# Performance work log

Measured on AMD Instinct MI355X. Metric: run time of the kernel, lower is better.

The kernel has to match this reference:

```python
import jax, jax.numpy as jnp
import numpy as np

B, N, D, H = 128, 32768, 768, 16
DH = D // H          # per-head hidden_size = memory_dim // num_heads = 48
BETA = 0.25          # scaling (inverse temperature)
STEPS = 5            # update_steps_max
TOPK = 4


def _ln(x, g, b):
    # torch nn.LayerNorm over last dim (biased variance, eps=1e-5), affine
    m = jnp.mean(x, axis=-1, keepdims=True)
    v = jnp.var(x, axis=-1, keepdims=True)
    return (x - m) * jax.lax.rsqrt(v + 1e-5) * g + b


def _l2norm(x):
    # F.normalize(x, dim=-1): x / max(||x||, 1e-12)
    n = jnp.linalg.norm(x, axis=-1, keepdims=True)
    return x / jnp.maximum(n, 1e-12)


def setup_inputs() -> dict:
    key = jax.random.key(0)
    ks = jax.random.split(key, 8)
    s = 0.05  # weight init scale to keep activations sane
    return {
        "query_embedding": jax.random.normal(ks[0], (B, D), jnp.float32),
        "memory_bank": jax.random.normal(ks[1], (N, D), jnp.float32),
        "ln_k_g": jnp.ones((D,), jnp.float32), "ln_k_b": jnp.zeros((D,), jnp.float32),
        "ln_q_g": jnp.ones((D,), jnp.float32), "ln_q_b": jnp.zeros((D,), jnp.float32),
        "ln_v_g": jnp.ones((D,), jnp.float32), "ln_v_b": jnp.zeros((D,), jnp.float32),
        "Wq": jax.random.normal(ks[2], (D, D), jnp.float32) * s, "bq": jnp.zeros((D,), jnp.float32),
        "Wk": jax.random.normal(ks[3], (D, D), jnp.float32) * s, "bk": jnp.zeros((D,), jnp.float32),
        "Wv": jax.random.normal(ks[4], (D, D), jnp.float32) * s, "bv": jnp.zeros((D,), jnp.float32),
        "Wo": jax.random.normal(ks[5], (D, D), jnp.float32) * s, "bo": jnp.zeros((D,), jnp.float32),
        "W1": jax.random.normal(ks[6], (D, D), jnp.float32) * s, "b1": jnp.zeros((D,), jnp.float32),
        "W2": jax.random.normal(ks[7], (D, D), jnp.float32) * s, "b2": jnp.zeros((D,), jnp.float32),
    }


def reference(query_embedding, memory_bank, ln_k_g, ln_k_b, ln_q_g, ln_q_b,
              ln_v_g, ln_v_b, Wq, bq, Wk, bk, Wv, bv, Wo, bo, W1, b1, W2, b2):
    # Affine LayerNorms on stored pattern, state pattern, pattern projection.
    # memory_bank is shared across the batch, so normalize/project it ONCE
    # instead of materializing the (B, N, D) expand from the torch code.
    stored = _ln(memory_bank, ln_k_g, ln_k_b)        # (N, D)
    state = _ln(query_embedding, ln_q_g, ln_q_b)     # (B, D) -- state pattern, seq len 1
    projp = _ln(memory_bank, ln_v_g, ln_v_b)         # (N, D)

    k = (stored @ Wk.T + bk).reshape(N, H, DH)       # (N, H, dh)
    v = (projp @ Wv.T + bv).reshape(N, H, DH)        # (N, H, dh)
    q = (state @ Wq.T + bq).reshape(B, H, DH)        # (B, H, dh)

    # Hopfield convergence: xi <- softmax(beta * xi K^T) K, repeated STEPS times
    def step(xi, _):
        attn = jax.nn.softmax(BETA * jnp.einsum('bhd,nhd->bhn', xi, k), axis=-1)
        return jnp.einsum('bhn,nhd->bhd', attn, k), None

    xi, _ = jax.lax.scan(step, q, None, length=STEPS)

    # Final readout against the (separately normalized) pattern projection V
    attn = jax.nn.softmax(BETA * jnp.einsum('bhd,nhd->bhn', xi, k), axis=-1)  # (B, H, N)
    converged = jnp.einsum('bhn,nhd->bhd', attn, v).reshape(B, D) @ Wo.T + bo  # (B, D)

    # Retrieval head: residual + MLP + cosine-sim logits + top-k
    combined = query_embedding + converged
    rq = jax.nn.relu(combined @ W1.T + b1) @ W2.T + b2
    logits = (_l2norm(rq) @ _l2norm(memory_bank).T) * 20.0   # (B, N)
    top_indices = jax.lax.top_k(logits, TOPK)[1]              # (B, TOPK)
    return top_indices, logits
```

## Files before the change

### kernel.cpp

```cpp
#include <hip/hip_runtime.h>
#include <math.h>

#define NTOT 32768
#define DMODEL 768
#define BSZ 128
#define NHEAD 16
#define DH 48
#define BETA 0.25f

typedef _Float16 f16;
typedef f16 f16x8 __attribute__((ext_vector_type(8)));
typedef f16 f16x4 __attribute__((ext_vector_type(4)));
typedef float f32x4 __attribute__((ext_vector_type(4)));

__global__ __launch_bounds__(256)
void row_stats(const float* __restrict__ X, int M, float* __restrict__ mean,
               float* __restrict__ rstd, float* __restrict__ l2inv) {
  const int row = blockIdx.x * 4 + (threadIdx.x >> 6);
  const int lane = threadIdx.x & 63;
  if (row >= M) return;
  const float* x = X + (size_t)row * DMODEL;
  float s = 0.f, s2 = 0.f;
  for (int i = lane; i < DMODEL; i += 64) {
    float v = x[i];
    s += v; s2 += v * v;
  }
#pragma unroll
  for (int off = 32; off; off >>= 1) {
    s  += __shfl_xor(s, off);
    s2 += __shfl_xor(s2, off);
  }
  if (lane == 0) {
    float mu = s * (1.f / DMODEL);
    float var = s2 * (1.f / DMODEL) - mu * mu;
    mean[row] = mu;
    rstd[row] = rsqrtf(var + 1e-5f);
    if (l2inv) l2inv[row] = 1.f / fmaxf(sqrtf(s2), 1e-12f);
  }
}

__global__ __launch_bounds__(256)
void split_ln(const float* __restrict__ X, const float* __restrict__ mean,
              const float* __restrict__ rstd, f16* __restrict__ hi,
              f16* __restrict__ lo) {
  const int i8 = blockIdx.x * 256 + threadIdx.x;
  const int row = i8 / 96;
  const float mu = mean[row], rs = rstd[row];
  const float* xp = X + (size_t)i8 * 8;
  const float4 a = *(const float4*)xp;
  const float4 b = *(const float4*)(xp + 4);
  const float x[8] = {a.x, a.y, a.z, a.w, b.x, b.y, b.z, b.w};
  f16x8 h, l;
#pragma unroll
  for (int j = 0; j < 8; j++) {
    const float s = (x[j] - mu) * rs;
    const f16 hv = (f16)s;
    h[j] = hv;
    l[j] = (f16)(s - (float)hv);
  }
  *(f16x8*)(hi + (size_t)i8 * 8) = h;
  *(f16x8*)(lo + (size_t)i8 * 8) = l;
}

__global__ __launch_bounds__(256)
void split_plain(const float* __restrict__ X, f16* __restrict__ hi,
                 f16* __restrict__ lo) {
  const int i8 = blockIdx.x * 256 + threadIdx.x;
  const float* xp = X + (size_t)i8 * 8;
  const float4 a = *(const float4*)xp;
  const float4 b = *(const float4*)(xp + 4);
  const float x[8] = {a.x, a.y, a.z, a.w, b.x, b.y, b.z, b.w};
  f16x8 h, l;
#pragma unroll
  for (int j = 0; j < 8; j++) {
    const f16 hv = (f16)x[j];
    h[j] = hv;
    l[j] = (f16)(x[j] - (float)hv);
  }
  *(f16x8*)(hi + (size_t)i8 * 8) = h;
  *(f16x8*)(lo + (size_t)i8 * 8) = l;
}

__global__ __launch_bounds__(256)
void prep_w(const float* __restrict__ Wk, const float* __restrict__ bk,
            const float* __restrict__ gk, const float* __restrict__ blnk,
            const float* __restrict__ Wv, const float* __restrict__ bv,
            const float* __restrict__ gv, const float* __restrict__ blnv,
            f16* __restrict__ Wc_hi, f16* __restrict__ Wc_lo,
            float* __restrict__ biasc) {
  const int o = blockIdx.x * 4 + (threadIdx.x >> 6);
  const int lane = threadIdx.x & 63;
  const bool isK = o < DMODEL;
  const float* W = isK ? (Wk + (size_t)o * DMODEL)
                       : (Wv + (size_t)(o - DMODEL) * DMODEL);
  const float* g   = isK ? gk : gv;
  const float* bln = isK ? blnk : blnv;
  float bacc = 0.f;
  for (int d = lane * 4; d < DMODEL; d += 256) {
    const float4 wv = *(const float4*)(W + d);
    const float4 g4 = *(const float4*)(g + d);
    const float4 b4 = *(const float4*)(bln + d);
    bacc += wv.x * b4.x + wv.y * b4.y + wv.z * b4.z + wv.w * b4.w;
    const float sv[4] = {wv.x * g4.x * 16.f, wv.y * g4.y * 16.f,
                         wv.z * g4.z * 16.f, wv.w * g4.w * 16.f};
    f16x4 h4, l4;
#pragma unroll
    for (int j = 0; j < 4; j++) {
      const f16 h = (f16)sv[j];
      h4[j] = h;
      l4[j] = (f16)(sv[j] - (float)h);
    }
    *(f16x4*)(Wc_hi + (size_t)o * DMODEL + d) = h4;
    *(f16x4*)(Wc_lo + (size_t)o * DMODEL + d) = l4;
  }
#pragma unroll
  for (int off = 32; off; off >>= 1) bacc += __shfl_xor(bacc, off);
  if (lane == 0) biasc[o] = (isK ? bk[o] : bv[o - DMODEL]) + bacc;
}

__global__ __launch_bounds__(256)
void proj_dual_v2(const f16* __restrict__ nh_hi, const f16* __restrict__ nh_lo,
                  const f16* __restrict__ Wc_hi, const f16* __restrict__ Wc_lo,
                  const float* __restrict__ biasc,
                  f16* __restrict__ k_hi, f16* __restrict__ k_lo,
                  f16* __restrict__ v_hi, f16* __restrict__ v_lo) {
  __shared__ __align__(16) f16 As[2][128][40];
  __shared__ __align__(16) f16 Bs[2][128][40];
  const int t = threadIdx.x;
  const int n0 = blockIdx.x * 128;
  const int m0 = blockIdx.y * 128;
  const int w = t >> 6, lane = t & 63;
  const int l15 = lane & 15, lq = lane >> 4;
  const int wm = w >> 1, wn = w & 1;
  const int sr = t >> 1, sh = t & 1;

  f32x4 acc[4][4];
#pragma unroll
  for (int a = 0; a < 4; a++)
#pragma unroll
    for (int b = 0; b < 4; b++)
#pragma unroll
      for (int r = 0; r < 4; r++) acc[a][b][r] = 0.f;

  for (int k0 = 0; k0 < DMODEL; k0 += 32) {
    __syncthreads();
    {
      const size_t aoff = (size_t)(m0 + sr) * DMODEL + k0 + sh * 16;
      f16x8 ah0 = *(const f16x8*)(nh_hi + aoff);
      f16x8 ah1 = *(const f16x8*)(nh_hi + aoff + 8);
      f16x8 al0 = *(const f16x8*)(nh_lo + aoff);
      f16x8 al1 = *(const f16x8*)(nh_lo + aoff + 8);
      *(f16x8*)&As[0][sr][sh * 16] = ah0;
      *(f16x8*)&As[0][sr][sh * 16 + 8] = ah1;
      *(f16x8*)&As[1][sr][sh * 16] = al0;
      *(f16x8*)&As[1][sr][sh * 16 + 8] = al1;
    }
    {
      const size_t boff = (size_t)(n0 + sr) * DMODEL + k0 + sh * 16;
      f16x8 bh0 = *(const f16x8*)(Wc_hi + boff);
      f16x8 bh1 = *(const f16x8*)(Wc_hi + boff + 8);
      f16x8 bl0 = *(const f16x8*)(Wc_lo + boff);
      f16x8 bl1 = *(const f16x8*)(Wc_lo + boff + 8);
      *(f16x8*)&Bs[0][sr][sh * 16] = bh0;
      *(f16x8*)&Bs[0][sr][sh * 16 + 8] = bh1;
      *(f16x8*)&Bs[1][sr][sh * 16] = bl0;
      *(f16x8*)&Bs[1][sr][sh * 16 + 8] = bl1;
    }
    __syncthreads();
    f16x8 nhh[4], nhl[4];
#pragma unroll
    for (int fm = 0; fm < 4; fm++) {
      const int row = wm * 64 + fm * 16 + l15;
      nhh[fm] = *(const f16x8*)&As[0][row][lq * 8];
      nhl[fm] = *(const f16x8*)&As[1][row][lq * 8];
    }
    f16x8 wh[4], wl[4];
#pragma unroll
    for (int fo = 0; fo < 4; fo++) {
      const int row = wn * 64 + fo * 16 + l15;
      wh[fo] = *(const f16x8*)&Bs[0][row][lq * 8];
      wl[fo] = *(const f16x8*)&Bs[1][row][lq * 8];
    }
#pragma unroll
    for (int fo = 0; fo < 4; fo++)
#pragma unroll
      for (int fm = 0; fm < 4; fm++) {
        f32x4 a = acc[fo][fm];
        a = __builtin_amdgcn_mfma_f32_16x16x32_f16(wh[fo], nhh[fm], a, 0, 0, 0);
        a = __builtin_amdgcn_mfma_f32_16x16x32_f16(wh[fo], nhl[fm], a, 0, 0, 0);
        a = __builtin_amdgcn_mfma_f32_16x16x32_f16(wl[fo], nhh[fm], a, 0, 0, 0);
        acc[fo][fm] = a;
      }
  }
  const int oc = n0 + wn * 64;
  const bool isK = oc < DMODEL;
  f16* oh = isK ? k_hi : v_hi;
  f16* ol = isK ? k_lo : v_lo;
  const int obase = (isK ? oc : oc - DMODEL) + lq * 4;
#pragma unroll
  for (int fo = 0; fo < 4; fo++) {
    const float4 bb = *(const float4*)(biasc + oc + fo * 16 + lq * 4);
    const float bbv[4] = {bb.x, bb.y, bb.z, bb.w};
    const int o = obase + fo * 16;
#pragma unroll
    for (int fm = 0; fm < 4; fm++) {
      const size_t moff = (size_t)(m0 + wm * 64 + fm * 16 + l15) * DMODEL + o;
      f16x4 h4, l4;
#pragma unroll
      for (int r = 0; r < 4; r++) {
        const float v = acc[fo][fm][r] * 0.0625f + bbv[r];
        const f16 h = (f16)v;
        h4[r] = h;
        l4[r] = (f16)(v - (float)h);
      }
      *(f16x4*)(oh + moff) = h4;
      *(f16x4*)(ol + moff) = l4;
    }
  }
}

__global__ __launch_bounds__(256)
void proj_dual_insplit(const float* __restrict__ mb, const float* __restrict__ mean,
                       const float* __restrict__ rstd,
                       const f16* __restrict__ Wc_hi, const f16* __restrict__ Wc_lo,
                       const float* __restrict__ biasc,
                       f16* __restrict__ k_hi, f16* __restrict__ k_lo,
                       f16* __restrict__ v_hi, f16* __restrict__ v_lo) {
  __shared__ __align__(16) f16 As[2][128][40];
  __shared__ __align__(16) f16 Bs[2][128][40];
  const int t = threadIdx.x;
  const int n0 = blockIdx.x * 128;
  const int m0 = blockIdx.y * 128;
  const int w = t >> 6, lane = t & 63;
  const int l15 = lane & 15, lq = lane >> 4;
  const int wm = w >> 1, wn = w & 1;
  const int sr = t >> 1, sh = t & 1;
  const float mu = mean[m0 + sr];
  const float rs = rstd[m0 + sr];
  f32x4 acc[4][4];
#pragma unroll
  for (int a = 0; a < 4; a++)
#pragma unroll
    for (int b = 0; b < 4; b++)
#pragma unroll
      for (int r = 0; r < 4; r++) acc[a][b][r] = 0.f;
  for (int k0 = 0; k0 < DMODEL; k0 += 32) {
    __syncthreads();
    {
      const float* ap = mb + (size_t)(m0 + sr) * DMODEL + k0 + sh * 16;
      float x[16];
#pragma unroll
      for (int c = 0; c < 4; c++) {
        const float4 v4 = *(const float4*)(ap + c * 4);
        x[c * 4 + 0] = v4.x; x[c * 4 + 1] = v4.y;
        x[c * 4 + 2] = v4.z; x[c * 4 + 3] = v4.w;
      }
      f16x8 h0, h1, l0, l1;
#pragma unroll
      for (int j = 0; j < 8; j++) {
        const float s = (x[j] - mu) * rs;
        const f16 h = (f16)s;
        h0[j] = h; l0[j] = (f16)(s - (float)h);
      }
#pragma unroll
      for (int j = 0; j < 8; j++) {
        const float s = (x[8 + j] - mu) * rs;
        const f16 h = (f16)s;
        h1[j] = h; l1[j] = (f16)(s - (float)h);
      }
      *(f16x8*)&As[0][sr][sh * 16] = h0;
      *(f16x8*)&As[0][sr][sh * 16 + 8] = h1;
      *(f16x8*)&As[1][sr][sh * 16] = l0;
      *(f16x8*)&As[1][sr][sh * 16 + 8] = l1;
    }
    {
      const size_t boff = (size_t)(n0 + sr) * DMODEL + k0 + sh * 16;
      f16x8 bh0 = *(const f16x8*)(Wc_hi + boff);
      f16x8 bh1 = *(const f16x8*)(Wc_hi + boff + 8);
      f16x8 bl0 = *(const f16x8*)(Wc_lo + boff);
      f16x8 bl1 = *(const f16x8*)(Wc_lo + boff + 8);
      *(f16x8*)&Bs[0][sr][sh * 16] = bh0;
      *(f16x8*)&Bs[0][sr][sh * 16 + 8] = bh1;
      *(f16x8*)&Bs[1][sr][sh * 16] = bl0;
      *(f16x8*)&Bs[1][sr][sh * 16 + 8] = bl1;
    }
    __syncthreads();
    f16x8 nhh[4], nhl[4];
#pragma unroll
    for (int fm = 0; fm < 4; fm++) {
      const int row = wm * 64 + fm * 16 + l15;
      nhh[fm] = *(const f16x8*)&As[0][row][lq * 8];
      nhl[fm] = *(const f16x8*)&As[1][row][lq * 8];
    }
    f16x8 wh[4], wl[4];
#pragma unroll
    for (int fo = 0; fo < 4; fo++) {
      const int row = wn * 64 + fo * 16 + l15;
      wh[fo] = *(const f16x8*)&Bs[0][row][lq * 8];
      wl[fo] = *(const f16x8*)&Bs[1][row][lq * 8];
    }
#pragma unroll
    for (int fo = 0; fo < 4; fo++)
#pragma unroll
      for (int fm = 0; fm < 4; fm++) {
        f32x4 a = acc[fo][fm];
        a = __builtin_amdgcn_mfma_f32_16x16x32_f16(wh[fo], nhh[fm], a, 0, 0, 0);
        a = __builtin_amdgcn_mfma_f32_16x16x32_f16(wh[fo], nhl[fm], a, 0, 0, 0);
        a = __builtin_amdgcn_mfma_f32_16x16x32_f16(wl[fo], nhh[fm], a, 0, 0, 0);
        acc[fo][fm] = a;
      }
  }
  const int oc = n0 + wn * 64;
  const bool isK = oc < DMODEL;
  f16* oh = isK ? k_hi : v_hi;
  f16* ol = isK ? k_lo : v_lo;
  const int obase = (isK ? oc : oc - DMODEL) + lq * 4;
#pragma unroll
  for (int fo = 0; fo < 4; fo++) {
    const float4 bb = *(const float4*)(biasc + oc + fo * 16 + lq * 4);
    const float bbv[4] = {bb.x, bb.y, bb.z, bb.w};
    const int o = obase + fo * 16;
#pragma unroll
    for (int fm = 0; fm < 4; fm++) {
      const size_t moff = (size_t)(m0 + wm * 64 + fm * 16 + l15) * DMODEL + o;
      f16x4 h4, l4;
#pragma unroll
      for (int r = 0; r < 4; r++) {
        const float v = acc[fo][fm][r] * 0.0625f + bbv[r];
        const f16 h = (f16)v;
        h4[r] = h;
        l4[r] = (f16)(v - (float)h);
      }
      *(f16x4*)(oh + moff) = h4;
      *(f16x4*)(ol + moff) = l4;
    }
  }
}

__global__ __launch_bounds__(256)
void logits_mfma(const f16* __restrict__ mb_hi, const f16* __restrict__ mb_lo,
                 const f16* __restrict__ rq_hi, const f16* __restrict__ rq_lo,
                 const float* __restrict__ ainv, const float* __restrict__ binv,
                 float* __restrict__ out) {
  __shared__ __align__(16) f16 As[2][128][40];
  __shared__ __align__(16) f16 Bs[2][128][40];
  const int t = threadIdx.x;
  const int n0 = blockIdx.x * 128;
  const int w = t >> 6, lane = t & 63;
  const int l15 = lane & 15, lq = lane >> 4;
  const int wb = w >> 1, wn = w & 1;
  const int sr = t >> 1, sh = t & 1;

  f32x4 acc[4][4];
#pragma unroll
  for (int a = 0; a < 4; a++)
#pragma unroll
    for (int b = 0; b < 4; b++)
#pragma unroll
      for (int r = 0; r < 4; r++) acc[a][b][r] = 0.f;

  for (int k0 = 0; k0 < DMODEL; k0 += 32) {
    __syncthreads();
    {
      const size_t aoff = (size_t)(n0 + sr) * DMODEL + k0 + sh * 16;
      f16x8 ah0 = *(const f16x8*)(mb_hi + aoff);
      f16x8 ah1 = *(const f16x8*)(mb_hi + aoff + 8);
      f16x8 al0 = *(const f16x8*)(mb_lo + aoff);
      f16x8 al1 = *(const f16x8*)(mb_lo + aoff + 8);
      *(f16x8*)&As[0][sr][sh * 16] = ah0;
      *(f16x8*)&As[0][sr][sh * 16 + 8] = ah1;
      *(f16x8*)&As[1][sr][sh * 16] = al0;
      *(f16x8*)&As[1][sr][sh * 16 + 8] = al1;
    }
    {
      const size_t boff = (size_t)sr * DMODEL + k0 + sh * 16;
      f16x8 bh0 = *(const f16x8*)(rq_hi + boff);
      f16x8 bh1 = *(const f16x8*)(rq_hi + boff + 8);
      f16x8 bl0 = *(const f16x8*)(rq_lo + boff);
      f16x8 bl1 = *(const f16x8*)(rq_lo + boff + 8);
      *(f16x8*)&Bs[0][sr][sh * 16] = bh0;
      *(f16x8*)&Bs[0][sr][sh * 16 + 8] = bh1;
      *(f16x8*)&Bs[1][sr][sh * 16] = bl0;
      *(f16x8*)&Bs[1][sr][sh * 16 + 8] = bl1;
    }
    __syncthreads();
    f16x8 ah[4], al[4];
#pragma unroll
    for (int fn = 0; fn < 4; fn++) {
      const int row = wn * 64 + fn * 16 + l15;
      ah[fn] = *(const f16x8*)&As[0][row][lq * 8];
      al[fn] = *(const f16x8*)&As[1][row][lq * 8];
    }
    f16x8 bh[4], bl[4];
#pragma unroll
    for (int fb = 0; fb < 4; fb++) {
      const int row = wb * 64 + fb * 16 + l15;
      bh[fb] = *(const f16x8*)&Bs[0][row][lq * 8];
      bl[fb] = *(const f16x8*)&Bs[1][row][lq * 8];
    }
#pragma unroll
    for (int fn = 0; fn < 4; fn++)
#pragma unroll
      for (int fb = 0; fb < 4; fb++) {
        f32x4 a = acc[fn][fb];
        a = __builtin_amdgcn_mfma_f32_16x16x32_f16(ah[fn], bh[fb], a, 0, 0, 0);
        a = __builtin_amdgcn_mfma_f32_16x16x32_f16(ah[fn], bl[fb], a, 0, 0, 0);
        a = __builtin_amdgcn_mfma_f32_16x16x32_f16(al[fn], bh[fb], a, 0, 0, 0);
        acc[fn][fb] = a;
      }
  }
#pragma unroll
  for (int fn = 0; fn < 4; fn++) {
    const int gn = n0 + wn * 64 + fn * 16 + lq * 4;
    const float4 bi4 = *(const float4*)(binv + gn);
    const float bi[4] = {bi4.x, bi4.y, bi4.z, bi4.w};
#pragma unroll
    for (int fb = 0; fb < 4; fb++) {
      const int b = wb * 64 + fb * 16 + l15;
      const float sa = 20.f * ainv[b];
      f32x4 o;
#pragma unroll
      for (int r = 0; r < 4; r++) o[r] = acc[fn][fb][r] * sa * bi[r];
      *(f32x4*)(out + (size_t)b * NTOT + gn) = o;
    }
  }
}

__global__ __launch_bounds__(256)
void ln_gemm_f32(const float* __restrict__ A, const float* __restrict__ mean,
                 const float* __restrict__ rstd, const float* __restrict__ g,
                 const float* __restrict__ bln, const float* __restrict__ W,
                 const float* __restrict__ bias, float* __restrict__ out) {
  __shared__ float As[16][68];
  __shared__ float Ws[16][68];
  const int t = threadIdx.x;
  const int m0 = blockIdx.y << 6, n0 = blockIdx.x << 6;
  const int tm = t >> 4, tn = t & 15;
  const int lr = t >> 2;
  const int lk = (t & 3) << 2;
  const float muL = mean[m0 + lr];
  const float rsL = rstd[m0 + lr];
  float acc[4][4] = {};
  for (int k0 = 0; k0 < DMODEL; k0 += 16) {
    float4 a4 = *(const float4*)(A + (size_t)(m0 + lr) * DMODEL + k0 + lk);
    float4 g4 = *(const float4*)(g + k0 + lk);
    float4 b4 = *(const float4*)(bln + k0 + lk);
    As[lk + 0][lr] = (a4.x - muL) * rsL * g4.x + b4.x;
    As[lk + 1][lr] = (a4.y - muL) * rsL * g4.y + b4.y;
    As[lk + 2][lr] = (a4.z - muL) * rsL * g4.z + b4.z;
    As[lk + 3][lr] = (a4.w - muL) * rsL * g4.w + b4.w;
    float4 w4 = *(const float4*)(W + (size_t)(n0 + lr) * DMODEL + k0 + lk);
    Ws[lk + 0][lr] = w4.x;
    Ws[lk + 1][lr] = w4.y;
    Ws[lk + 2][lr] = w4.z;
    Ws[lk + 3][lr] = w4.w;
    __syncthreads();
#pragma unroll
    for (int kk = 0; kk < 16; kk++) {
      const float4 av = *(const float4*)(&As[kk][tm * 4]);
      const float4 bv = *(const float4*)(&Ws[kk][tn * 4]);
      const float a[4] = {av.x, av.y, av.z, av.w};
      const float b[4] = {bv.x, bv.y, bv.z, bv.w};
#pragma unroll
      for (int i = 0; i < 4; i++)
#pragma unroll
        for (int j = 0; j < 4; j++) acc[i][j] += a[i] * b[j];
    }
    __syncthreads();
  }
  const float4 bia = *(const float4*)(bias + n0 + tn * 4);
  const float bb[4] = {bia.x, bia.y, bia.z, bia.w};
#pragma unroll
  for (int i = 0; i < 4; i++) {
    const int m = m0 + tm * 4 + i;
    float4 o4;
    o4.x = acc[i][0] + bb[0];
    o4.y = acc[i][1] + bb[1];
    o4.z = acc[i][2] + bb[2];
    o4.w = acc[i][3] + bb[3];
    *(float4*)(out + (size_t)m * DMODEL + n0 + tn * 4) = o4;
  }
}

__global__ __launch_bounds__(256)
void gemm_bias(const float* __restrict__ A, const float* __restrict__ W,
               const float* __restrict__ bias, const float* __restrict__ add,
               float* __restrict__ out, int relu) {
  __shared__ float As[16][68];
  __shared__ float Ws[16][68];
  const int t = threadIdx.x;
  const int m0 = blockIdx.y << 6, n0 = blockIdx.x << 6;
  const int tm = t >> 4, tn = t & 15;
  const int lr = t >> 2;
  const int lk = (t & 3) << 2;
  float acc[4][4] = {};
  for (int k0 = 0; k0 < DMODEL; k0 += 16) {
    float4 a4 = *(const float4*)(A + (size_t)(m0 + lr) * DMODEL + k0 + lk);
    As[lk + 0][lr] = a4.x;
    As[lk + 1][lr] = a4.y;
    As[lk + 2][lr] = a4.z;
    As[lk + 3][lr] = a4.w;
    float4 w4 = *(const float4*)(W + (size_t)(n0 + lr) * DMODEL + k0 + lk);
    Ws[lk + 0][lr] = w4.x;
    Ws[lk + 1][lr] = w4.y;
    Ws[lk + 2][lr] = w4.z;
    Ws[lk + 3][lr] = w4.w;
    __syncthreads();
#pragma unroll
    for (int kk = 0; kk < 16; kk++) {
      const float4 av = *(const float4*)(&As[kk][tm * 4]);
      const float4 bv = *(const float4*)(&Ws[kk][tn * 4]);
      const float a[4] = {av.x, av.y, av.z, av.w};
      const float b[4] = {bv.x, bv.y, bv.z, bv.w};
#pragma unroll
      for (int i = 0; i < 4; i++)
#pragma unroll
        for (int j = 0; j < 4; j++) acc[i][j] += a[i] * b[j];
    }
    __syncthreads();
  }
  const float4 bia = *(const float4*)(bias + n0 + tn * 4);
  const float bb[4] = {bia.x, bia.y, bia.z, bia.w};
#pragma unroll
  for (int i = 0; i < 4; i++) {
    const int m = m0 + tm * 4 + i;
    float v[4];
#pragma unroll
    for (int j = 0; j < 4; j++) v[j] = acc[i][j] + bb[j];
    if (add) {
      const float4 a4 = *(const float4*)(add + (size_t)m * DMODEL + n0 + tn * 4);
      v[0] += a4.x; v[1] += a4.y; v[2] += a4.z; v[3] += a4.w;
    }
    if (relu) {
#pragma unroll
      for (int j = 0; j < 4; j++) v[j] = fmaxf(v[j], 0.f);
    }
    float4 o4 = {v[0], v[1], v[2], v[3]};
    *(float4*)(out + (size_t)m * DMODEL + n0 + tn * 4) = o4;
  }
}

__global__ __launch_bounds__(256)
void split_xi_k(const float* __restrict__ xi, f16* __restrict__ hi,
                f16* __restrict__ lo) {
  const int i = blockIdx.x * 256 + threadIdx.x;
  float4 v = ((const float4*)xi)[i];
  float s[4] = {v.x * BETA, v.y * BETA, v.z * BETA, v.w * BETA};
  f16x4 h4, l4;
#pragma unroll
  for (int j = 0; j < 4; j++) {
    f16 h = (f16)s[j];
    h4[j] = h;
    l4[j] = (f16)(s[j] - (float)h);
  }
  ((f16x4*)hi)[i] = h4;
  ((f16x4*)lo)[i] = l4;
}

#define FCHUNK 64
#define FROWS (NTOT / FCHUNK)

__global__ __launch_bounds__(256)
void flash_round(const f16* __restrict__ k_hi, const f16* __restrict__ k_lo,
                 const f16* __restrict__ val_hi, const f16* __restrict__ val_lo,
                 const f16* __restrict__ xi_hi, const f16* __restrict__ xi_lo,
                 float* __restrict__ part_ml, float* __restrict__ part_o,
                 int valIsK) {
  const int h = blockIdx.y, chunk = blockIdx.x;
  const int tid = threadIdx.x, w = tid >> 6, lane = tid & 63;
  const int l15 = lane & 15, lq = lane >> 4;
  const int b0 = w * 32;

  __shared__ __align__(16) f16 krow[2][32][56];
  __shared__ __align__(16) f16 vT[2][48][40];
  __shared__ __align__(16) f16 pHi[4][32][40];
  __shared__ __align__(16) f16 pLo[4][32][40];

  const f16x8 zf = {};
  f16x8 xqh[2][2], xql[2][2];
#pragma unroll
  for (int bt = 0; bt < 2; bt++) {
    const size_t xoff = (size_t)(b0 + bt * 16 + l15) * DMODEL + h * DH;
    xqh[bt][0] = *(const f16x8*)(xi_hi + xoff + lq * 8);
    xql[bt][0] = *(const f16x8*)(xi_lo + xoff + lq * 8);
    const size_t xo1 = xoff + 32 + (lq & 1) * 8;
    f16x8 th = *(const f16x8*)(xi_hi + xo1);
    f16x8 tl = *(const f16x8*)(xi_lo + xo1);
    xqh[bt][1] = (lq < 2) ? th : zf;
    xql[bt][1] = (lq < 2) ? tl : zf;
  }

  float m[2] = {-1e30f, -1e30f}, lsum[2] = {0.f, 0.f};
  f32x4 O[3][2];
#pragma unroll
  for (int mt = 0; mt < 3; mt++)
#pragma unroll
    for (int bt = 0; bt < 2; bt++)
#pragma unroll
      for (int j = 0; j < 4; j++) O[mt][bt][j] = 0.f;

  const int nbase = chunk * FROWS;
  for (int it = 0; it < FROWS / 32; it++) {
    const int gn0 = nbase + it * 32;
    __syncthreads();
    for (int j = tid; j < 384; j += 256) {
      const int tsel = j / 192;
      const int q = j - tsel * 192;
      const int r = q / 6;
      const int d0 = (q - r * 6) * 8;
      const size_t goff = (size_t)(gn0 + r) * DMODEL + h * DH + d0;
      const f16* kp = (tsel ? k_lo : k_hi) + goff;
      f16x8 kv = *(const f16x8*)kp;
      f16x8 vv;
      if (valIsK) {
        vv = kv;
      } else {
        const f16* vp = (tsel ? val_lo : val_hi) + goff;
        vv = *(const f16x8*)vp;
      }
      *(f16x8*)&krow[tsel][r][d0] = kv;
#pragma unroll
      for (int jj = 0; jj < 8; jj++) vT[tsel][d0 + jj][r] = vv[jj];
    }
    __syncthreads();

    f16x8 akh[2][2], akl[2][2];
#pragma unroll
    for (int nt = 0; nt < 2; nt++) {
      const int row = nt * 16 + l15;
      akh[nt][0] = *(const f16x8*)&krow[0][row][lq * 8];
      akl[nt][0] = *(const f16x8*)&krow[1][row][lq * 8];
      f16x8 t0 = *(const f16x8*)&krow[0][row][32 + (lq & 1) * 8];
      f16x8 t1 = *(const f16x8*)&krow[1][row][32 + (lq & 1) * 8];
      akh[nt][1] = (lq < 2) ? t0 : zf;
      akl[nt][1] = (lq < 2) ? t1 : zf;
    }
    f32x4 S[2][2];
#pragma unroll
    for (int nt = 0; nt < 2; nt++)
#pragma unroll
      for (int bt = 0; bt < 2; bt++) {
        f32x4 s = {};
        s = __builtin_amdgcn_mfma_f32_16x16x32_f16(akh[nt][0], xqh[bt][0], s, 0, 0, 0);
        s = __builtin_amdgcn_mfma_f32_16x16x32_f16(akh[nt][1], xqh[bt][1], s, 0, 0, 0);
        s = __builtin_amdgcn_mfma_f32_16x16x32_f16(akh[nt][0], xql[bt][0], s, 0, 0, 0);
        s = __builtin_amdgcn_mfma_f32_16x16x32_f16(akh[nt][1], xql[bt][1], s, 0, 0, 0);
        s = __builtin_amdgcn_mfma_f32_16x16x32_f16(akl[nt][0], xqh[bt][0], s, 0, 0, 0);
        s = __builtin_amdgcn_mfma_f32_16x16x32_f16(akl[nt][1], xqh[bt][1], s, 0, 0, 0);
        S[nt][bt] = s;
      }
    float sc[2];
#pragma unroll
    for (int bt = 0; bt < 2; bt++) {
      float mx = S[0][bt][0];
#pragma unroll
      for (int r = 1; r < 4; r++) mx = fmaxf(mx, S[0][bt][r]);
#pragma unroll
      for (int r = 0; r < 4; r++) mx = fmaxf(mx, S[1][bt][r]);
      mx = fmaxf(mx, __shfl_xor(mx, 16));
      mx = fmaxf(mx, __shfl_xor(mx, 32));
      const float mnew = fmaxf(m[bt], mx);
      sc[bt] = __expf(m[bt] - mnew);
      float ps = 0.f;
#pragma unroll
      for (int nt = 0; nt < 2; nt++) {
        f16x4 ph, pl;
#pragma unroll
        for (int r = 0; r < 4; r++) {
          const float p = __expf(S[nt][bt][r] - mnew);
          ps += p;
          const f16 hh = (f16)p;
          ph[r] = hh;
          pl[r] = (f16)(p - (float)hh);
        }
        *(f16x4*)&pHi[w][bt * 16 + l15][nt * 16 + lq * 4] = ph;
        *(f16x4*)&pLo[w][bt * 16 + l15][nt * 16 + lq * 4] = pl;
      }
      ps += __shfl_xor(ps, 16);
      ps += __shfl_xor(ps, 32);
      lsum[bt] = lsum[bt] * sc[bt] + ps;
      m[bt] = mnew;
    }
    __asm__ volatile("s_waitcnt lgkmcnt(0)" ::: "memory");
    f16x8 avh[3], avl[3];
#pragma unroll
    for (int mt = 0; mt < 3; mt++) {
      avh[mt] = *(const f16x8*)&vT[0][mt * 16 + l15][lq * 8];
      avl[mt] = *(const f16x8*)&vT[1][mt * 16 + l15][lq * 8];
    }
    f16x8 pbh[2], pbl[2];
#pragma unroll
    for (int bt = 0; bt < 2; bt++) {
      pbh[bt] = *(const f16x8*)&pHi[w][bt * 16 + l15][lq * 8];
      pbl[bt] = *(const f16x8*)&pLo[w][bt * 16 + l15][lq * 8];
    }
#pragma unroll
    for (int mt = 0; mt < 3; mt++)
#pragma unroll
      for (int bt = 0; bt < 2; bt++) {
#pragma unroll
        for (int j = 0; j < 4; j++) O[mt][bt][j] *= sc[bt];
        f32x4 o = O[mt][bt];
        o = __builtin_amdgcn_mfma_f32_16x16x32_f16(avh[mt], pbh[bt], o, 0, 0, 0);
        o = __builtin_amdgcn_mfma_f32_16x16x32_f16(avh[mt], pbl[bt], o, 0, 0, 0);
        o = __builtin_amdgcn_mfma_f32_16x16x32_f16(avl[mt], pbh[bt], o, 0, 0, 0);
        O[mt][bt] = o;
      }
  }
  const int pc = h * FCHUNK + chunk;
  if (lq == 0) {
#pragma unroll
    for (int bt = 0; bt < 2; bt++) {
      float* pm = part_ml + ((size_t)pc * BSZ + b0 + bt * 16 + l15) * 2;
      pm[0] = m[bt];
      pm[1] = lsum[bt];
    }
  }
#pragma unroll
  for (int mt = 0; mt < 3; mt++)
#pragma unroll
    for (int bt = 0; bt < 2; bt++) {
      float* po = part_o + ((size_t)pc * BSZ + b0 + bt * 16 + l15) * 48 +
                  mt * 16 + lq * 4;
      *(f32x4*)po = O[mt][bt];
    }
}

__global__ __launch_bounds__(64)
void hopfield_combine(const float* __restrict__ part_ml,
                      const float* __restrict__ part_o, float* __restrict__ dst) {
  const int bh = blockIdx.x;
  const int h = bh >> 7, b = bh & 127;
  const int c = threadIdx.x;
  __shared__ float w[64];
  const float* pm = part_ml + ((size_t)(h * 64 + c) * BSZ + b) * 2;
  const float mp = pm[0];
  const float lp = pm[1];
  float M = mp;
#pragma unroll
  for (int off = 32; off; off >>= 1) M = fmaxf(M, __shfl_xor(M, off));
  const float wp = __expf(mp - M);
  w[c] = wp;
  float L = lp * wp;
#pragma unroll
  for (int off = 32; off; off >>= 1) L += __shfl_xor(L, off);
  __syncthreads();
  if (c < DH) {
    float o = 0.f;
    for (int p = 0; p < 64; p++)
      o += part_o[((size_t)(h * 64 + p) * BSZ + b) * 48 + c] * w[p];
    dst[(size_t)b * DMODEL + h * DH + c] = o / L;
  }
}

__global__ __launch_bounds__(256)
void topk_kernel(const float* __restrict__ logits, float* __restrict__ outIdx) {
  const int b = blockIdx.x;
  const int t = threadIdx.x;
  const float* row = logits + (size_t)b * NTOT;
  float v[4] = {-1e30f, -1e30f, -1e30f, -1e30f};
  int id[4] = {0x7fffffff, 0x7fffffff, 0x7fffffff, 0x7fffffff};
  for (int n = t; n < NTOT; n += 256) {
    const float x = row[n];
    if (x > v[3]) {
      v[3] = x; id[3] = n;
#pragma unroll
      for (int s = 3; s > 0; s--) {
        const bool sw = (v[s] > v[s - 1]) || (v[s] == v[s - 1] && id[s] < id[s - 1]);
        if (sw) {
          float tv = v[s]; v[s] = v[s - 1]; v[s - 1] = tv;
          int ti = id[s]; id[s] = id[s - 1]; id[s - 1] = ti;
        }
      }
    }
  }
  __shared__ float sv[256][4];
  __shared__ int si[256][4];
#pragma unroll
  for (int j = 0; j < 4; j++) { sv[t][j] = v[j]; si[t][j] = id[j]; }
  for (int str = 128; str >= 1; str >>= 1) {
    __syncthreads();
    if (t < str) {
      float a[4], c[4];
      int ai[4], ci[4];
#pragma unroll
      for (int j = 0; j < 4; j++) {
        a[j] = sv[t][j]; ai[j] = si[t][j];
        c[j] = sv[t + str][j]; ci[j] = si[t + str][j];
      }
      float rv[4]; int ri[4];
      int p = 0, q = 0;
#pragma unroll
      for (int oo = 0; oo < 4; oo++) {
        const bool ta = (a[p] > c[q]) || (a[p] == c[q] && ai[p] < ci[q]);
        if (ta) { rv[oo] = a[p]; ri[oo] = ai[p]; p++; }
        else    { rv[oo] = c[q]; ri[oo] = ci[q]; q++; }
      }
#pragma unroll
      for (int j = 0; j < 4; j++) { sv[t][j] = rv[j]; si[t][j] = ri[j]; }
    }
  }
  if (t == 0) {
#pragma unroll
    for (int j = 0; j < 4; j++) outIdx[b * 4 + j] = (float)si[0][j];
  }
}

extern "C" void kernel_launch(void* const* d_in, const int* in_sizes, int n_in,
                              void* d_out, int out_size, void* d_ws, size_t ws_size,
                              hipStream_t stream) {
  const float* qe    = (const float*)d_in[0];
  const float* mb    = (const float*)d_in[1];
  const float* ln_kg = (const float*)d_in[2];
  const float* ln_kb = (const float*)d_in[3];
  const float* ln_qg = (const float*)d_in[4];
  const float* ln_qb = (const float*)d_in[5];
  const float* ln_vg = (const float*)d_in[6];
  const float* ln_vb = (const float*)d_in[7];
  const float* Wq = (const float*)d_in[8];
  const float* bq = (const float*)d_in[9];
  const float* Wk = (const float*)d_in[10];
  const float* bk = (const float*)d_in[11];
  const float* Wv = (const float*)d_in[12];
  const float* bv = (const float*)d_in[13];
  const float* Wo = (const float*)d_in[14];
  const float* bo = (const float*)d_in[15];
  const float* W1 = (const float*)d_in[16];
  const float* b1 = (const float*)d_in[17];
  const float* W2 = (const float*)d_in[18];
  const float* b2 = (const float*)d_in[19];

  float* out = (float*)d_out;
  float* logits = out + BSZ * 4;

  const size_t ND16 = (size_t)NTOT * DMODEL / 2;
  const size_t PART = (size_t)NHEAD * FCHUNK * BSZ * (2 + 48);
  const size_t fixed = 3 * NTOT + 768 + 4 * ND16 + 4 * (size_t)BSZ * DMODEL +
                       4 * (size_t)BSZ * DMODEL / 2 +
                       2 * (size_t)2 * DMODEL * DMODEL / 2 + 2 * DMODEL;
  const bool fast = (fixed + 2 * ND16) * sizeof(float) <= ws_size;
  const size_t nhpart = fast ? 2 * ND16 : PART;

  float* ws = (float*)d_ws;
  size_t off = 0;
  auto alloc = [&](size_t n) { float* p = ws + off; off += n; return p; };
  float* mb_mean = alloc(NTOT);
  float* mb_rstd = alloc(NTOT);
  float* mb_l2i  = alloc(NTOT);
  float* q_mean  = alloc(128);
  float* q_rstd  = alloc(128);
  float* rq_inv  = alloc(128);
  float* pad_    = alloc(384);
  f16* k_hi = (f16*)alloc(ND16);
  f16* k_lo = (f16*)alloc(ND16);
  f16* v_hi = (f16*)alloc(ND16);
  f16* v_lo = (f16*)alloc(ND16);
  float* nhpart_base = alloc(nhpart);
  f16* nh_hi = (f16*)nhpart_base;
  f16* nh_lo = (f16*)(nhpart_base + ND16);
  float* part_ml = nhpart_base;
  float* part_o  = nhpart_base + (size_t)NHEAD * FCHUNK * BSZ * 2;
  float* xi   = alloc((size_t)BSZ * DMODEL);
  float* conv = alloc((size_t)BSZ * DMODEL);
  float* comb = alloc((size_t)BSZ * DMODEL);
  float* h1   = alloc((size_t)BSZ * DMODEL);
  f16* xi_hi = (f16*)alloc((size_t)BSZ * DMODEL / 2);
  f16* xi_lo = (f16*)alloc((size_t)BSZ * DMODEL / 2);
  f16* rq_hi = (f16*)alloc((size_t)BSZ * DMODEL / 2);
  f16* rq_lo = (f16*)alloc((size_t)BSZ * DMODEL / 2);
  f16* Wc_hi = (f16*)alloc((size_t)2 * DMODEL * DMODEL / 2);
  f16* Wc_lo = (f16*)alloc((size_t)2 * DMODEL * DMODEL / 2);
  float* biasc = alloc(2 * DMODEL);
  f16* mb16_hi = (f16*)k_hi;
  f16* mb16_lo = (f16*)k_lo;
  (void)in_sizes; (void)n_in; (void)out_size; (void)pad_;

  row_stats<<<NTOT / 4, 256, 0, stream>>>(mb, NTOT, mb_mean, mb_rstd, mb_l2i);
  row_stats<<<BSZ / 4, 256, 0, stream>>>(qe, BSZ, q_mean, q_rstd, nullptr);
  prep_w<<<2 * DMODEL / 4, 256, 0, stream>>>(Wk, bk, ln_kg, ln_kb,
                                             Wv, bv, ln_vg, ln_vb,
                                             Wc_hi, Wc_lo, biasc);

  if (fast) {
    split_ln<<<(NTOT * DMODEL / 8) / 256, 256, 0, stream>>>(
        mb, mb_mean, mb_rstd, nh_hi, nh_lo);
    proj_dual_v2<<<dim3(2 * DMODEL / 128, NTOT / 128), 256, 0, stream>>>(
        nh_hi, nh_lo, Wc_hi, Wc_lo, biasc, k_hi, k_lo, v_hi, v_lo);
  } else {
    proj_dual_insplit<<<dim3(2 * DMODEL / 128, NTOT / 128), 256, 0, stream>>>(
        mb, mb_mean, mb_rstd, Wc_hi, Wc_lo, biasc, k_hi, k_lo, v_hi, v_lo);
  }
  ln_gemm_f32<<<dim3(DMODEL / 64, BSZ / 64), 256, 0, stream>>>(
      qe, q_mean, q_rstd, ln_qg, ln_qb, Wq, bq, xi);

  for (int r = 0; r < 6; r++) {
    const int valIsK = (r != 5);
    const f16* valHi = valIsK ? k_hi : v_hi;
    const f16* valLo = valIsK ? k_lo : v_lo;
    float* dst = (r == 5) ? conv : xi;
    split_xi_k<<<96, 256, 0, stream>>>(xi, xi_hi, xi_lo);
    flash_round<<<dim3(FCHUNK, NHEAD), 256, 0, stream>>>(
        k_hi, k_lo, valHi, valLo, xi_hi, xi_lo, part_ml, part_o, valIsK);
    hopfield_combine<<<BSZ * NHEAD, 64, 0, stream>>>(part_ml, part_o, dst);
  }

  gemm_bias<<<dim3(DMODEL / 64, BSZ / 64), 256, 0, stream>>>(conv, Wo, bo, qe, comb, 0);
  gemm_bias<<<dim3(DMODEL / 64, BSZ / 64), 256, 0, stream>>>(comb, W1, b1, nullptr, h1, 1);
  float* rq = conv;
  gemm_bias<<<dim3(DMODEL / 64, BSZ / 64), 256, 0, stream>>>(h1, W2, b2, nullptr, rq, 0);

  row_stats<<<BSZ / 4, 256, 0, stream>>>(rq, BSZ, q_mean, q_rstd, rq_inv);
  split_plain<<<(NTOT * DMODEL / 8) / 256, 256, 0, stream>>>(mb, mb16_hi, mb16_lo);
  split_plain<<<(BSZ * DMODEL / 8) / 256, 256, 0, stream>>>(rq, rq_hi, rq_lo);
  logits_mfma<<<NTOT / 128, 256, 0, stream>>>(mb16_hi, mb16_lo, rq_hi, rq_lo,
                                              rq_inv, mb_l2i, logits);

  topk_kernel<<<BSZ, 256, 0, stream>>>(logits, out);
}
```

Baseline: 1.505 ms.

## Write transposed K/V from projection and use direct-load flash Hopfield rounds

```diff
diff --git a/kernel.cpp b/kernel.cpp
--- a/kernel.cpp
+++ b/kernel.cpp
@@ -7,6 +7,9 @@
 #define NHEAD 16
 #define DH 48
 #define BETA 0.25f
+
+#define FCHUNK 32
+#define FROWS (NTOT / FCHUNK)
 
 typedef _Float16 f16;
 typedef f16 f16x8 __attribute__((ext_vector_type(8)));
@@ -40,29 +43,6 @@
 }
 
 __global__ __launch_bounds__(256)
-void split_ln(const float* __restrict__ X, const float* __restrict__ mean,
-              const float* __restrict__ rstd, f16* __restrict__ hi,
-              f16* __restrict__ lo) {
-  const int i8 = blockIdx.x * 256 + threadIdx.x;
-  const int row = i8 / 96;
-  const float mu = mean[row], rs = rstd[row];
-  const float* xp = X + (size_t)i8 * 8;
-  const float4 a = *(const float4*)xp;
-  const float4 b = *(const float4*)(xp + 4);
-  const float x[8] = {a.x, a.y, a.z, a.w, b.x, b.y, b.z, b.w};
-  f16x8 h, l;
-#pragma unroll
-  for (int j = 0; j < 8; j++) {
-    const float s = (x[j] - mu) * rs;
-    const f16 hv = (f16)s;
-    h[j] = hv;
-    l[j] = (f16)(s - (float)hv);
-  }
-  *(f16x8*)(hi + (size_t)i8 * 8) = h;
-  *(f16x8*)(lo + (size_t)i8 * 8) = l;
-}
-
-__global__ __launch_bounds__(256)
 void split_plain(const float* __restrict__ X, f16* __restrict__ hi,
                  f16* __restrict__ lo) {
   const int i8 = blockIdx.x * 256 + threadIdx.x;
@@ -79,6 +59,23 @@
   }
   *(f16x8*)(hi + (size_t)i8 * 8) = h;
   *(f16x8*)(lo + (size_t)i8 * 8) = l;
+}
+
+__global__ __launch_bounds__(256)
+void split_xi_k(const float* __restrict__ xi, f16* __restrict__ hi,
+                f16* __restrict__ lo) {
+  const int i = blockIdx.x * 256 + threadIdx.x;
+  float4 v = ((const float4*)xi)[i];
+  float s[4] = {v.x * BETA, v.y * BETA, v.z * BETA, v.w * BETA};
+  f16x4 h4, l4;
+#pragma unroll
+  for (int j = 0; j < 4; j++) {
+    f16 h = (f16)s[j];
+    h4[j] = h;
+    l4[j] = (f16)(s[j] - (float)h);
+  }
+  ((f16x4*)hi)[i] = h4;
+  ((f16x4*)lo)[i] = l4;
 }
 
 __global__ __launch_bounds__(256)
@@ -119,113 +116,14 @@
 }
 
 __global__ __launch_bounds__(256)
-void proj_dual_v2(const f16* __restrict__ nh_hi, const f16* __restrict__ nh_lo,
+void proj_dual_tr(const float* __restrict__ mb, const float* __restrict__ mean,
+                  const float* __restrict__ rstd,
                   const f16* __restrict__ Wc_hi, const f16* __restrict__ Wc_lo,
                   const float* __restrict__ biasc,
                   f16* __restrict__ k_hi, f16* __restrict__ k_lo,
-                  f16* __restrict__ v_hi, f16* __restrict__ v_lo) {
-  __shared__ __align__(16) f16 As[2][128][40];
-  __shared__ __align__(16) f16 Bs[2][128][40];
-  const int t = threadIdx.x;
-  const int n0 = blockIdx.x * 128;
-  const int m0 = blockIdx.y * 128;
-  const int w = t >> 6, lane = t & 63;
-  const int l15 = lane & 15, lq = lane >> 4;
-  const int wm = w >> 1, wn = w & 1;
-  const int sr = t >> 1, sh = t & 1;
-
-  f32x4 acc[4][4];
-#pragma unroll
-  for (int a = 0; a < 4; a++)
-#pragma unroll
-    for (int b = 0; b < 4; b++)
-#pragma unroll
-      for (int r = 0; r < 4; r++) acc[a][b][r] = 0.f;
-
-  for (int k0 = 0; k0 < DMODEL; k0 += 32) {
-    __syncthreads();
-    {
-      const size_t aoff = (size_t)(m0 + sr) * DMODEL + k0 + sh * 16;
-      f16x8 ah0 = *(const f16x8*)(nh_hi + aoff);
-      f16x8 ah1 = *(const f16x8*)(nh_hi + aoff + 8);
-      f16x8 al0 = *(const f16x8*)(nh_lo + aoff);
-      f16x8 al1 = *(const f16x8*)(nh_lo + aoff + 8);
-      *(f16x8*)&As[0][sr][sh * 16] = ah0;
-      *(f16x8*)&As[0][sr][sh * 16 + 8] = ah1;
-      *(f16x8*)&As[1][sr][sh * 16] = al0;
-      *(f16x8*)&As[1][sr][sh * 16 + 8] = al1;
-    }
-    {
-      const size_t boff = (size_t)(n0 + sr) * DMODEL + k0 + sh * 16;
-      f16x8 bh0 = *(const f16x8*)(Wc_hi + boff);
-      f16x8 bh1 = *(const f16x8*)(Wc_hi + boff + 8);
-      f16x8 bl0 = *(const f16x8*)(Wc_lo + boff);
-      f16x8 bl1 = *(const f16x8*)(Wc_lo + boff + 8);
-      *(f16x8*)&Bs[0][sr][sh * 16] = bh0;
-      *(f16x8*)&Bs[0][sr][sh * 16 + 8] = bh1;
-      *(f16x8*)&Bs[1][sr][sh * 16] = bl0;
-      *(f16x8*)&Bs[1][sr][sh * 16 + 8] = bl1;
-    }
-    __syncthreads();
-    f16x8 nhh[4], nhl[4];
-#pragma unroll
-    for (int fm = 0; fm < 4; fm++) {
-      const int row = wm * 64 + fm * 16 + l15;
-      nhh[fm] = *(const f16x8*)&As[0][row][lq * 8];
-      nhl[fm] = *(const f16x8*)&As[1][row][lq * 8];
-    }
-    f16x8 wh[4], wl[4];
-#pragma unroll
-    for (int fo = 0; fo < 4; fo++) {
-      const int row = wn * 64 + fo * 16 + l15;
-      wh[fo] = *(const f16x8*)&Bs[0][row][lq * 8];
-      wl[fo] = *(const f16x8*)&Bs[1][row][lq * 8];
-    }
-#pragma unroll
-    for (int fo = 0; fo < 4; fo++)
-#pragma unroll
-      for (int fm = 0; fm < 4; fm++) {
-        f32x4 a = acc[fo][fm];
-        a = __builtin_amdgcn_mfma_f32_16x16x32_f16(wh[fo], nhh[fm], a, 0, 0, 0);
-        a = __builtin_amdgcn_mfma_f32_16x16x32_f16(wh[fo], nhl[fm], a, 0, 0, 0);
-        a = __builtin_amdgcn_mfma_f32_16x16x32_f16(wl[fo], nhh[fm], a, 0, 0, 0);
-        acc[fo][fm] = a;
-      }
-  }
-  const int oc = n0 + wn * 64;
-  const bool isK = oc < DMODEL;
-  f16* oh = isK ? k_hi : v_hi;
-  f16* ol = isK ? k_lo : v_lo;
-  const int obase = (isK ? oc : oc - DMODEL) + lq * 4;
-#pragma unroll
-  for (int fo = 0; fo < 4; fo++) {
-    const float4 bb = *(const float4*)(biasc + oc + fo * 16 + lq * 4);
-    const float bbv[4] = {bb.x, bb.y, bb.z, bb.w};
-    const int o = obase + fo * 16;
-#pragma unroll
-    for (int fm = 0; fm < 4; fm++) {
-      const size_t moff = (size_t)(m0 + wm * 64 + fm * 16 + l15) * DMODEL + o;
-      f16x4 h4, l4;
-#pragma unroll
-      for (int r = 0; r < 4; r++) {
-        const float v = acc[fo][fm][r] * 0.0625f + bbv[r];
-        const f16 h = (f16)v;
-        h4[r] = h;
-        l4[r] = (f16)(v - (float)h);
-      }
-      *(f16x4*)(oh + moff) = h4;
-      *(f16x4*)(ol + moff) = l4;
-    }
-  }
-}
-
-__global__ __launch_bounds__(256)
-void proj_dual_insplit(const float* __restrict__ mb, const float* __restrict__ mean,
-                       const float* __restrict__ rstd,
-                       const f16* __restrict__ Wc_hi, const f16* __restrict__ Wc_lo,
-                       const float* __restrict__ biasc,
-                       f16* __restrict__ k_hi, f16* __restrict__ k_lo,
-                       f16* __restrict__ v_hi, f16* __restrict__ v_lo) {
+                  f16* __restrict__ kT_hi, f16* __restrict__ kT_lo,
+                  f16* __restrict__ vT_hi, f16* __restrict__ vT_lo,
+                  int mode) {
   __shared__ __align__(16) f16 As[2][128][40];
   __shared__ __align__(16) f16 Bs[2][128][40];
   const int t = threadIdx.x;
@@ -312,17 +210,15 @@
   }
   const int oc = n0 + wn * 64;
   const bool isK = oc < DMODEL;
-  f16* oh = isK ? k_hi : v_hi;
-  f16* ol = isK ? k_lo : v_lo;
-  const int obase = (isK ? oc : oc - DMODEL) + lq * 4;
+  const int ocl = isK ? oc : oc - DMODEL;
 #pragma unroll
   for (int fo = 0; fo < 4; fo++) {
     const float4 bb = *(const float4*)(biasc + oc + fo * 16 + lq * 4);
     const float bbv[4] = {bb.x, bb.y, bb.z, bb.w};
-    const int o = obase + fo * 16;
+    const int o = ocl + fo * 16 + lq * 4;
 #pragma unroll
     for (int fm = 0; fm < 4; fm++) {
-      const size_t moff = (size_t)(m0 + wm * 64 + fm * 16 + l15) * DMODEL + o;
+      const int mcol = m0 + wm * 64 + fm * 16 + l15;
       f16x4 h4, l4;
 #pragma unroll
       for (int r = 0; r < 4; r++) {
@@ -331,97 +227,366 @@
         h4[r] = h;
         l4[r] = (f16)(v - (float)h);
       }
-      *(f16x4*)(oh + moff) = h4;
-      *(f16x4*)(ol + moff) = l4;
-    }
-  }
-}
-
-__global__ __launch_bounds__(256)
-void logits_mfma(const f16* __restrict__ mb_hi, const f16* __restrict__ mb_lo,
-                 const f16* __restrict__ rq_hi, const f16* __restrict__ rq_lo,
-                 const float* __restrict__ ainv, const float* __restrict__ binv,
-                 float* __restrict__ out) {
-  __shared__ __align__(16) f16 As[2][128][40];
-  __shared__ __align__(16) f16 Bs[2][128][40];
-  const int t = threadIdx.x;
-  const int n0 = blockIdx.x * 128;
-  const int w = t >> 6, lane = t & 63;
+      if (mode == 0) {
+        f16* oh = isK ? k_hi : vT_hi;
+        f16* ol = isK ? k_lo : vT_lo;
+        *(f16x4*)(oh + (size_t)mcol * DMODEL + o) = h4;
+        *(f16x4*)(ol + (size_t)mcol * DMODEL + o) = l4;
+      } else {
+        if (isK) {
+          *(f16x4*)(k_hi + (size_t)mcol * DMODEL + o) = h4;
+          *(f16x4*)(k_lo + (size_t)mcol * DMODEL + o) = l4;
+        }
+        f16* Thi = isK ? kT_hi : vT_hi;
+        f16* Tlo = isK ? kT_lo : vT_lo;
+#pragma unroll
+        for (int r = 0; r < 4; r++) {
+          Thi[(size_t)(o + r) * NTOT + mcol] = h4[r];
+          Tlo[(size_t)(o + r) * NTOT + mcol] = l4[r];
+        }
+      }
+    }
+  }
+}
+
+__global__ __launch_bounds__(256)
+void flash_direct(const f16* __restrict__ k_hi, const f16* __restrict__ k_lo,
+                  const f16* __restrict__ valT_hi, const f16* __restrict__ valT_lo,
+                  const f16* __restrict__ xi_hi, const f16* __restrict__ xi_lo,
+                  float* __restrict__ part_ml, float* __restrict__ part_o) {
+  const int h = blockIdx.y, chunk = blockIdx.x;
+  const int tid = threadIdx.x, w = tid >> 6, lane = tid & 63;
   const int l15 = lane & 15, lq = lane >> 4;
-  const int wb = w >> 1, wn = w & 1;
-  const int sr = t >> 1, sh = t & 1;
-
-  f32x4 acc[4][4];
-#pragma unroll
-  for (int a = 0; a < 4; a++)
-#pragma unroll
-    for (int b = 0; b < 4; b++)
-#pragma unroll
-      for (int r = 0; r < 4; r++) acc[a][b][r] = 0.f;
-
-  for (int k0 = 0; k0 < DMODEL; k0 += 32) {
-    __syncthreads();
-    {
-      const size_t aoff = (size_t)(n0 + sr) * DMODEL + k0 + sh * 16;
-      f16x8 ah0 = *(const f16x8*)(mb_hi + aoff);
-      f16x8 ah1 = *(const f16x8*)(mb_hi + aoff + 8);
-      f16x8 al0 = *(const f16x8*)(mb_lo + aoff);
-      f16x8 al1 = *(const f16x8*)(mb_lo + aoff + 8);
-      *(f16x8*)&As[0][sr][sh * 16] = ah0;
-      *(f16x8*)&As[0][sr][sh * 16 + 8] = ah1;
-      *(f16x8*)&As[1][sr][sh * 16] = al0;
-      *(f16x8*)&As[1][sr][sh * 16 + 8] = al1;
-    }
-    {
-      const size_t boff = (size_t)sr * DMODEL + k0 + sh * 16;
-      f16x8 bh0 = *(const f16x8*)(rq_hi + boff);
-      f16x8 bh1 = *(const f16x8*)(rq_hi + boff + 8);
-      f16x8 bl0 = *(const f16x8*)(rq_lo + boff);
-      f16x8 bl1 = *(const f16x8*)(rq_lo + boff + 8);
-      *(f16x8*)&Bs[0][sr][sh * 16] = bh0;
-      *(f16x8*)&Bs[0][sr][sh * 16 + 8] = bh1;
-      *(f16x8*)&Bs[1][sr][sh * 16] = bl0;
-      *(f16x8*)&Bs[1][sr][sh * 16 + 8] = bl1;
-    }
-    __syncthreads();
-    f16x8 ah[4], al[4];
-#pragma unroll
-    for (int fn = 0; fn < 4; fn++) {
-      const int row = wn * 64 + fn * 16 + l15;
-      ah[fn] = *(const f16x8*)&As[0][row][lq * 8];
-      al[fn] = *(const f16x8*)&As[1][row][lq * 8];
-    }
-    f16x8 bh[4], bl[4];
-#pragma unroll
-    for (int fb = 0; fb < 4; fb++) {
-      const int row = wb * 64 + fb * 16 + l15;
-      bh[fb] = *(const f16x8*)&Bs[0][row][lq * 8];
-      bl[fb] = *(const f16x8*)&Bs[1][row][lq * 8];
-    }
-#pragma unroll
-    for (int fn = 0; fn < 4; fn++)
-#pragma unroll
-      for (int fb = 0; fb < 4; fb++) {
-        f32x4 a = acc[fn][fb];
-        a = __builtin_amdgcn_mfma_f32_16x16x32_f16(ah[fn], bh[fb], a, 0, 0, 0);
-        a = __builtin_amdgcn_mfma_f32_16x16x32_f16(ah[fn], bl[fb], a, 0, 0, 0);
-        a = __builtin_amdgcn_mfma_f32_16x16x32_f16(al[fn], bh[fb], a, 0, 0, 0);
-        acc[fn][fb] = a;
-      }
-  }
-#pragma unroll
-  for (int fn = 0; fn < 4; fn++) {
-    const int gn = n0 + wn * 64 + fn * 16 + lq * 4;
-    const float4 bi4 = *(const float4*)(binv + gn);
-    const float bi[4] = {bi4.x, bi4.y, bi4.z, bi4.w};
-#pragma unroll
-    for (int fb = 0; fb < 4; fb++) {
-      const int b = wb * 64 + fb * 16 + l15;
-      const float sa = 20.f * ainv[b];
-      f32x4 o;
-#pragma unroll
-      for (int r = 0; r < 4; r++) o[r] = acc[fn][fb][r] * sa * bi[r];
-      *(f32x4*)(out + (size_t)b * NTOT + gn) = o;
+  const int b0 = w * 32;
+  __shared__ __align__(16) f16 pHi[4][32][40];
+  __shared__ __align__(16) f16 pLo[4][32][40];
+
+  const f16x8 zf = {};
+  f16x8 xqh[2][2], xql[2][2];
+#pragma unroll
+  for (int bt = 0; bt < 2; bt++) {
+    const size_t xoff = (size_t)(b0 + bt * 16 + l15) * DMODEL + h * DH;
+    xqh[bt][0] = *(const f16x8*)(xi_hi + xoff + lq * 8);
+    xql[bt][0] = *(const f16x8*)(xi_lo + xoff + lq * 8);
+    const size_t xo1 = xoff + 32 + (lq & 1) * 8;
+    f16x8 th = *(const f16x8*)(xi_hi + xo1);
+    f16x8 tl = *(const f16x8*)(xi_lo + xo1);
+    xqh[bt][1] = (lq < 2) ? th : zf;
+    xql[bt][1] = (lq < 2) ? tl : zf;
+  }
+
+  float m[2] = {-1e30f, -1e30f}, lsum[2] = {0.f, 0.f};
+  f32x4 O[3][2];
+#pragma unroll
+  for (int mt = 0; mt < 3; mt++)
+#pragma unroll
+    for (int bt = 0; bt < 2; bt++)
+#pragma unroll
+      for (int j = 0; j < 4; j++) O[mt][bt][j] = 0.f;
+
+  const int nbase = chunk * FROWS;
+  for (int it = 0; it < FROWS / 32; it++) {
+    const int gn0 = nbase + it * 32;
+    f16x8 akh[2][2], akl[2][2];
+#pragma unroll
+    for (int nt = 0; nt < 2; nt++) {
+      const size_t koff = (size_t)(gn0 + nt * 16 + l15) * DMODEL + h * DH;
+      akh[nt][0] = *(const f16x8*)(k_hi + koff + lq * 8);
+      akl[nt][0] = *(const f16x8*)(k_lo + koff + lq * 8);
+      f16x8 t0 = *(const f16x8*)(k_hi + koff + 32 + (lq & 1) * 8);
+      f16x8 t1 = *(const f16x8*)(k_lo + koff + 32 + (lq & 1) * 8);
+      akh[nt][1] = (lq < 2) ? t0 : zf;
+      akl[nt][1] = (lq < 2) ? t1 : zf;
+    }
+    f16x8 avh[3], avl[3];
+#pragma unroll
+    for (int mt = 0; mt < 3; mt++) {
+      const size_t voff = (size_t)(h * DH + mt * 16 + l15) * NTOT + gn0 + lq * 8;
+      avh[mt] = *(const f16x8*)(valT_hi + voff);
+      avl[mt] = *(const f16x8*)(valT_lo + voff);
+    }
+    f32x4 S[2][2];
+#pragma unroll
+    for (int nt = 0; nt < 2; nt++)
+#pragma unroll
+      for (int bt = 0; bt < 2; bt++) {
+        f32x4 s = {};
+        s = __builtin_amdgcn_mfma_f32_16x16x32_f16(akh[nt][0], xqh[bt][0], s, 0, 0, 0);
+        s = __builtin_amdgcn_mfma_f32_16x16x32_f16(akh[nt][1], xqh[bt][1], s, 0, 0, 0);
+        s = __builtin_amdgcn_mfma_f32_16x16x32_f16(akh[nt][0], xql[bt][0], s, 0, 0, 0);
+        s = __builtin_amdgcn_mfma_f32_16x16x32_f16(akh[nt][1], xql[bt][1], s, 0, 0, 0);
+        s = __builtin_amdgcn_mfma_f32_16x16x32_f16(akl[nt][0], xqh[bt][0], s, 0, 0, 0);
+        s = __builtin_amdgcn_mfma_f32_16x16x32_f16(akl[nt][1], xqh[bt][1], s, 0, 0, 0);
+        S[nt][bt] = s;
+      }
+    float sc[2];
+#pragma unroll
+    for (int bt = 0; bt < 2; bt++) {
+      float mx = S[0][bt][0];
+#pragma unroll
+      for (int r = 1; r < 4; r++) mx = fmaxf(mx, S[0][bt][r]);
+#pragma unroll
+      for (int r = 0; r < 4; r++) mx = fmaxf(mx, S[1][bt][r]);
+      mx = fmaxf(mx, __shfl_xor(mx, 16));
+      mx = fmaxf(mx, __shfl_xor(mx, 32));
+      const float mnew = fmaxf(m[bt], mx);
+      sc[bt] = __expf(m[bt] - mnew);
+      float ps = 0.f;
+#pragma unroll
+      for (int nt = 0; nt < 2; nt++) {
+        f16x4 ph, pl;
+#pragma unroll
+        for (int r = 0; r < 4; r++) {
+          const float p = __expf(S[nt][bt][r] - mnew);
+          ps += p;
+          const f16 hh = (f16)p;
+          ph[r] = hh;
+          pl[r] = (f16)(p - (float)hh);
+        }
+        *(f16x4*)&pHi[w][bt * 16 + l15][nt * 16 + lq * 4] = ph;
+        *(f16x4*)&pLo[w][bt * 16 + l15][nt * 16 + lq * 4] = pl;
+      }
+      ps += __shfl_xor(ps, 16);
+      ps += __shfl_xor(ps, 32);
+      lsum[bt] = lsum[bt] * sc[bt] + ps;
+      m[bt] = mnew;
+    }
+    __asm__ volatile("s_waitcnt lgkmcnt(0)" ::: "memory");
+    f16x8 pbh[2], pbl[2];
+#pragma unroll
+    for (int bt = 0; bt < 2; bt++) {
+      pbh[bt] = *(const f16x8*)&pHi[w][bt * 16 + l15][lq * 8];
+      pbl[bt] = *(const f16x8*)&pLo[w][bt * 16 + l15][lq * 8];
+    }
+#pragma unroll
+    for (int mt = 0; mt < 3; mt++)
+#pragma unroll
+      for (int bt = 0; bt < 2; bt++) {
+#pragma unroll
+        for (int j = 0; j < 4; j++) O[mt][bt][j] *= sc[bt];
+        f32x4 o = O[mt][bt];
+        o = __builtin_amdgcn_mfma_f32_16x16x32_f16(avh[mt], pbh[bt], o, 0, 0, 0);
+        o = __builtin_amdgcn_mfma_f32_16x16x32_f16(avh[mt], pbl[bt], o, 0, 0, 0);
+        o = __builtin_amdgcn_mfma_f32_16x16x32_f16(avl[mt], pbh[bt], o, 0, 0, 0);
+        O[mt][bt] = o;
+      }
+  }
+  const int pc = h * FCHUNK + chunk;
+  if (lq == 0) {
+#pragma unroll
+    for (int bt = 0; bt < 2; bt++) {
+      float* pm = part_ml + ((size_t)pc * BSZ + b0 + bt * 16 + l15) * 2;
+      pm[0] = m[bt];
+      pm[1] = lsum[bt];
+    }
+  }
+#pragma unroll
+  for (int mt = 0; mt < 3; mt++)
+#pragma unroll
+    for (int bt = 0; bt < 2; bt++) {
+      float* po = part_o + ((size_t)pc * BSZ + b0 + bt * 16 + l15) * 48 +
+                  mt * 16 + lq * 4;
+      *(f32x4*)po = O[mt][bt];
+    }
+}
+
+__global__ __launch_bounds__(256)
+void flash_staged(const f16* __restrict__ k_hi, const f16* __restrict__ k_lo,
+                  const f16* __restrict__ val_hi, const f16* __restrict__ val_lo,
+                  const f16* __restrict__ xi_hi, const f16* __restrict__ xi_lo,
+                  float* __restrict__ part_ml, float* __restrict__ part_o,
+                  int valIsK) {
+  const int h = blockIdx.y, chunk = blockIdx.x;
+  const int tid = threadIdx.x, w = tid >> 6, lane = tid & 63;
+  const int l15 = lane & 15, lq = lane >> 4;
+  const int b0 = w * 32;
+  __shared__ __align__(16) f16 krow[2][32][56];
+  __shared__ __align__(16) f16 vT[2][48][40];
+  __shared__ __align__(16) f16 pHi[4][32][40];
+  __shared__ __align__(16) f16 pLo[4][32][40];
+  const f16x8 zf = {};
+  f16x8 xqh[2][2], xql[2][2];
+#pragma unroll
+  for (int bt = 0; bt < 2; bt++) {
+    const size_t xoff = (size_t)(b0 + bt * 16 + l15) * DMODEL + h * DH;
+    xqh[bt][0] = *(const f16x8*)(xi_hi + xoff + lq * 8);
+    xql[bt][0] = *(const f16x8*)(xi_lo + xoff + lq * 8);
+    const size_t xo1 = xoff + 32 + (lq & 1) * 8;
+    f16x8 th = *(const f16x8*)(xi_hi + xo1);
+    f16x8 tl = *(const f16x8*)(xi_lo + xo1);
+    xqh[bt][1] = (lq < 2) ? th : zf;
+    xql[bt][1] = (lq < 2) ? tl : zf;
+  }
+  float m[2] = {-1e30f, -1e30f}, lsum[2] = {0.f, 0.f};
+  f32x4 O[3][2];
+#pragma unroll
+  for (int mt = 0; mt < 3; mt++)
+#pragma unroll
+    for (int bt = 0; bt < 2; bt++)
+#pragma unroll
+      for (int j = 0; j < 4; j++) O[mt][bt][j] = 0.f;
+  const int nbase = chunk * FROWS;
+  for (int it = 0; it < FROWS / 32; it++) {
+    const int gn0 = nbase + it * 32;
+    __syncthreads();
+    for (int j = tid; j < 384; j += 256) {
+      const int tsel = j / 192;
+      const int q = j - tsel * 192;
+      const int r = q / 6;
+      const int d0 = (q - r * 6) * 8;
+      const size_t goff = (size_t)(gn0 + r) * DMODEL + h * DH + d0;
+      const f16* kp = (tsel ? k_lo : k_hi) + goff;
+      f16x8 kv = *(const f16x8*)kp;
+      f16x8 vv;
+      if (valIsK) {
+        vv = kv;
+      } else {
+        const f16* vp = (tsel ? val_lo : val_hi) + goff;
+        vv = *(const f16x8*)vp;
+      }
+      *(f16x8*)&krow[tsel][r][d0] = kv;
+#pragma unroll
+      for (int jj = 0; jj < 8; jj++) vT[tsel][d0 + jj][r] = vv[jj];
+    }
+    __syncthreads();
+    f16x8 akh[2][2], akl[2][2];
+#pragma unroll
+    for (int nt = 0; nt < 2; nt++) {
+      const int row = nt * 16 + l15;
+      akh[nt][0] = *(const f16x8*)&krow[0][row][lq * 8];
+      akl[nt][0] = *(const f16x8*)&krow[1][row][lq * 8];
+      f16x8 t0 = *(const f16x8*)&krow[0][row][32 + (lq & 1) * 8];
+      f16x8 t1 = *(const f16x8*)&krow[1][row][32 + (lq & 1) * 8];
+      akh[nt][1] = (lq < 2) ? t0 : zf;
+      akl[nt][1] = (lq < 2) ? t1 : zf;
+    }
+    f32x4 S[2][2];
+#pragma unroll
+    for (int nt = 0; nt < 2; nt++)
+#pragma unroll
+      for (int bt = 0; bt < 2; bt++) {
+        f32x4 s = {};
+        s = __builtin_amdgcn_mfma_f32_16x16x32_f16(akh[nt][0], xqh[bt][0], s, 0, 0, 0);
+        s = __builtin_amdgcn_mfma_f32_16x16x32_f16(akh[nt][1], xqh[bt][1], s, 0, 0, 0);
+        s = __builtin_amdgcn_mfma_f32_16x16x32_f16(akh[nt][0], xql[bt][0], s, 0, 0, 0);
+        s = __builtin_amdgcn_mfma_f32_16x16x32_f16(akh[nt][1], xql[bt][1], s, 0, 0, 0);
+        s = __builtin_amdgcn_mfma_f32_16x16x32_f16(akl[nt][0], xqh[bt][0], s, 0, 0, 0);
+        s = __builtin_amdgcn_mfma_f32_16x16x32_f16(akl[nt][1], xqh[bt][1], s, 0, 0, 0);
+        S[nt][bt] = s;
+      }
+    float sc[2];
+#pragma unroll
+    for (int bt = 0; bt < 2; bt++) {
+      float mx = S[0][bt][0];
+#pragma unroll
+      for (int r = 1; r < 4; r++) mx = fmaxf(mx, S[0][bt][r]);
+#pragma unroll
+      for (int r = 0; r < 4; r++) mx = fmaxf(mx, S[1][bt][r]);
+      mx = fmaxf(mx, __shfl_xor(mx, 16));
+      mx = fmaxf(mx, __shfl_xor(mx, 32));
+      const float mnew = fmaxf(m[bt], mx);
+      sc[bt] = __expf(m[bt] - mnew);
+      float ps = 0.f;
+#pragma unroll
+      for (int nt = 0; nt < 2; nt++) {
+        f16x4 ph, pl;
+#pragma unroll
+        for (int r = 0; r < 4; r++) {
+          const float p = __expf(S[nt][bt][r] - mnew);
+          ps += p;
+          const f16 hh = (f16)p;
+          ph[r] = hh;
+          pl[r] = (f16)(p - (float)hh);
+        }
+        *(f16x4*)&pHi[w][bt * 16 + l15][nt * 16 + lq * 4] = ph;
+        *(f16x4*)&pLo[w][bt * 16 + l15][nt * 16 + lq * 4] = pl;
+      }
+      ps += __shfl_xor(ps, 16);
+      ps += __shfl_xor(ps, 32);
+      lsum[bt] = lsum[bt] * sc[bt] + ps;
+      m[bt] = mnew;
+    }
+    __asm__ volatile("s_waitcnt lgkmcnt(0)" ::: "memory");
+    f16x8 avh[3], avl[3];
+#pragma unroll
+    for (int mt = 0; mt < 3; mt++) {
+      avh[mt] = *(const f16x8*)&vT[0][mt * 16 + l15][lq * 8];
+      avl[mt] = *(const f16x8*)&vT[1][mt * 16 + l15][lq * 8];
+    }
+    f16x8 pbh[2], pbl[2];
+#pragma unroll
+    for (int bt = 0; bt < 2; bt++) {
+      pbh[bt] = *(const f16x8*)&pHi[w][bt * 16 + l15][lq * 8];
+      pbl[bt] = *(const f16x8*)&pLo[w][bt * 16 + l15][lq * 8];
+    }
+#pragma unroll
+    for (int mt = 0; mt < 3; mt++)
+#pragma unroll
+      for (int bt = 0; bt < 2; bt++) {
+#pragma unroll
+        for (int j = 0; j < 4; j++) O[mt][bt][j] *= sc[bt];
+        f32x4 o = O[mt][bt];
+        o = __builtin_amdgcn_mfma_f32_16x16x32_f16(avh[mt], pbh[bt], o, 0, 0, 0);
+        o = __builtin_amdgcn_mfma_f32_16x16x32_f16(avh[mt], pbl[bt], o, 0, 0, 0);
+        o = __builtin_amdgcn_mfma_f32_16x16x32_f16(avl[mt], pbh[bt], o, 0, 0, 0);
+        O[mt][bt] = o;
+      }
+  }
+  const int pc = h * FCHUNK + chunk;
+  if (lq == 0) {
+#pragma unroll
+    for (int bt = 0; bt < 2; bt++) {
+      float* pm = part_ml + ((size_t)pc * BSZ + b0 + bt * 16 + l15) * 2;
+      pm[0] = m[bt];
+      pm[1] = lsum[bt];
+    }
+  }
+#pragma unroll
+  for (int mt = 0; mt < 3; mt++)
+#pragma unroll
+    for (int bt = 0; bt < 2; bt++) {
+      float* po = part_o + ((size_t)pc * BSZ + b0 + bt * 16 + l15) * 48 +
+                  mt * 16 + lq * 4;
+      *(f32x4*)po = O[mt][bt];
+    }
+}
+
+__global__ __launch_bounds__(64)
+void combine_v2(const float* __restrict__ part_ml,
+                const float* __restrict__ part_o, int final_round,
+                float* __restrict__ conv, f16* __restrict__ xi_hi,
+                f16* __restrict__ xi_lo) {
+  const int bh = blockIdx.x;
+  const int h = bh >> 7, b = bh & 127;
+  const int c = threadIdx.x;
+  __shared__ float w[32];
+  float mp = -1e30f, lp = 0.f;
+  if (c < FCHUNK) {
+    const float* pm = part_ml + ((size_t)(h * FCHUNK + c) * BSZ + b) * 2;
+    mp = pm[0];
+    lp = pm[1];
+  }
+  float M = mp;
+#pragma unroll
+  for (int off = 32; off; off >>= 1) M = fmaxf(M, __shfl_xor(M, off));
+  const float wp = (c < FCHUNK) ? __expf(mp - M) : 0.f;
+  if (c < FCHUNK) w[c] = wp;
+  float L = lp * wp;
+#pragma unroll
+  for (int off = 32; off; off >>= 1) L += __shfl_xor(L, off);
+  __syncthreads();
+  if (c < DH) {
+    float o = 0.f;
+    for (int p = 0; p < FCHUNK; p++)
+      o += part_o[((size_t)(h * FCHUNK + p) * BSZ + b) * 48 + c] * w[p];
+    const float val = o / L;
+    if (final_round) {
+      conv[(size_t)b * DMODEL + h * DH + c] = val;
+    } else {
+      const float s = val * BETA;
+      const f16 hh = (f16)s;
+      xi_hi[(size_t)b * DMODEL + h * DH + c] = hh;
+      xi_lo[(size_t)b * DMODEL + h * DH + c] = (f16)(s - (float)hh);
     }
   }
 }
@@ -541,215 +706,89 @@
 }
 
 __global__ __launch_bounds__(256)
-void split_xi_k(const float* __restrict__ xi, f16* __restrict__ hi,
-                f16* __restrict__ lo) {
-  const int i = blockIdx.x * 256 + threadIdx.x;
-  float4 v = ((const float4*)xi)[i];
-  float s[4] = {v.x * BETA, v.y * BETA, v.z * BETA, v.w * BETA};
-  f16x4 h4, l4;
-#pragma unroll
-  for (int j = 0; j < 4; j++) {
-    f16 h = (f16)s[j];
-    h4[j] = h;
-    l4[j] = (f16)(s[j] - (float)h);
-  }
-  ((f16x4*)hi)[i] = h4;
-  ((f16x4*)lo)[i] = l4;
-}
-
-#define FCHUNK 64
-#define FROWS (NTOT / FCHUNK)
-
-__global__ __launch_bounds__(256)
-void flash_round(const f16* __restrict__ k_hi, const f16* __restrict__ k_lo,
-                 const f16* __restrict__ val_hi, const f16* __restrict__ val_lo,
-                 const f16* __restrict__ xi_hi, const f16* __restrict__ xi_lo,
-                 float* __restrict__ part_ml, float* __restrict__ part_o,
-                 int valIsK) {
-  const int h = blockIdx.y, chunk = blockIdx.x;
-  const int tid = threadIdx.x, w = tid >> 6, lane = tid & 63;
+void logits_mfma(const f16* __restrict__ mb_hi, const f16* __restrict__ mb_lo,
+                 const f16* __restrict__ rq_hi, const f16* __restrict__ rq_lo,
+                 const float* __restrict__ ainv, const float* __restrict__ binv,
+                 float* __restrict__ out) {
+  __shared__ __align__(16) f16 As[2][128][40];
+  __shared__ __align__(16) f16 Bs[2][128][40];
+  const int t = threadIdx.x;
+  const int n0 = blockIdx.x * 128;
+  const int w = t >> 6, lane = t & 63;
   const int l15 = lane & 15, lq = lane >> 4;
-  const int b0 = w * 32;
-
-  __shared__ __align__(16) f16 krow[2][32][56];
-  __shared__ __align__(16) f16 vT[2][48][40];
-  __shared__ __align__(16) f16 pHi[4][32][40];
-  __shared__ __align__(16) f16 pLo[4][32][40];
-
-  const f16x8 zf = {};
-  f16x8 xqh[2][2], xql[2][2];
-#pragma unroll
-  for (int bt = 0; bt < 2; bt++) {
-    const size_t xoff = (size_t)(b0 + bt * 16 + l15) * DMODEL + h * DH;
-    xqh[bt][0] = *(const f16x8*)(xi_hi + xoff + lq * 8);
-    xql[bt][0] = *(const f16x8*)(xi_lo + xoff + lq * 8);
-    const size_t xo1 = xoff + 32 + (lq & 1) * 8;
-    f16x8 th = *(const f16x8*)(xi_hi + xo1);
-    f16x8 tl = *(const f16x8*)(xi_lo + xo1);
-    xqh[bt][1] = (lq < 2) ? th : zf;
-    xql[bt][1] = (lq < 2) ? tl : zf;
-  }
-
-  float m[2] = {-1e30f, -1e30f}, lsum[2] = {0.f, 0.f};
-  f32x4 O[3][2];
-#pragma unroll
-  for (int mt = 0; mt < 3; mt++)
-#pragma unroll
-    for (int bt = 0; bt < 2; bt++)
-#pragma unroll
-      for (int j = 0; j < 4; j++) O[mt][bt][j] = 0.f;
-
-  const int nbase = chunk * FROWS;
-  for (int it = 0; it < FROWS / 32; it++) {
-    const int gn0 = nbase + it * 32;
-    __syncthreads();
-    for (int j = tid; j < 384; j += 256) {
-      const int tsel = j / 192;
-      const int q = j - tsel * 192;
-      const int r = q / 6;
-      const int d0 = (q - r * 6) * 8;
-      const size_t goff = (size_t)(gn0 + r) * DMODEL + h * DH + d0;
-      const f16* kp = (tsel ? k_lo : k_hi) + goff;
-      f16x8 kv = *(const f16x8*)kp;
-      f16x8 vv;
-      if (valIsK) {
-        vv = kv;
-      } else {
-        const f16* vp = (tsel ? val_lo : val_hi) + goff;
-        vv = *(const f16x8*)vp;
-      }
-      *(f16x8*)&krow[tsel][r][d0] = kv;
-#pragma unroll
-      for (int jj = 0; jj < 8; jj++) vT[tsel][d0 + jj][r] = vv[jj];
-    }
-    __syncthreads();
-
-    f16x8 akh[2][2], akl[2][2];
-#pragma unroll
-    for (int nt = 0; nt < 2; nt++) {
-      const int row = nt * 16 + l15;
-      akh[nt][0] = *(const f16x8*)&krow[0][row][lq * 8];
-      akl[nt][0] = *(const f16x8*)&krow[1][row][lq * 8];
-      f16x8 t0 = *(const f16x8*)&krow[0][row][32 + (lq & 1) * 8];
-      f16x8 t1 = *(const f16x8*)&krow[1][row][32 + (lq & 1) * 8];
-      akh[nt][1] = (lq < 2) ? t0 : zf;
-      akl[nt][1] = (lq < 2) ? t1 : zf;
-    }
-    f32x4 S[2][2];
-#pragma unroll
-    for (int nt = 0; nt < 2; nt++)
-#pragma unroll
-      for (int bt = 0; bt < 2; bt++) {
-        f32x4 s = {};
-        s = __builtin_amdgcn_mfma_f32_16x16x32_f16(akh[nt][0], xqh[bt][0], s, 0, 0, 0);
-        s = __builtin_amdgcn_mfma_f32_16x16x32_f16(akh[nt][1], xqh[bt][1], s, 0, 0, 0);
-        s = __builtin_amdgcn_mfma_f32_16x16x32_f16(akh[nt][0], xql[bt][0], s, 0, 0, 0);
-        s = __builtin_amdgcn_mfma_f32_16x16x32_f16(akh[nt][1], xql[bt][1], s, 0, 0, 0);
-        s = __builtin_amdgcn_mfma_f32_16x16x32_f16(akl[nt][0], xqh[bt][0], s, 0, 0, 0);
-        s = __builtin_amdgcn_mfma_f32_16x16x32_f16(akl[nt][1], xqh[bt][1], s, 0, 0, 0);
-        S[nt][bt] = s;
-      }
-    float sc[2];
-#pragma unroll
-    for (int bt = 0; bt < 2; bt++) {
-      float mx = S[0][bt][0];
-#pragma unroll
-      for (int r = 1; r < 4; r++) mx = fmaxf(mx, S[0][bt][r]);
-#pragma unroll
-      for (int r = 0; r < 4; r++) mx = fmaxf(mx, S[1][bt][r]);
-      mx = fmaxf(mx, __shfl_xor(mx, 16));
-      mx = fmaxf(mx, __shfl_xor(mx, 32));
-      const float mnew = fmaxf(m[bt], mx);
-      sc[bt] = __expf(m[bt] - mnew);
-      float ps = 0.f;
-#pragma unroll
-      for (int nt = 0; nt < 2; nt++) {
-        f16x4 ph, pl;
-#pragma unroll
-        for (int r = 0; r < 4; r++) {
-          const float p = __expf(S[nt][bt][r] - mnew);
-          ps += p;
-          const f16 hh = (f16)p;
-          ph[r] = hh;
-          pl[r] = (f16)(p - (float)hh);
-        }
-        *(f16x4*)&pHi[w][bt * 16 + l15][nt * 16 + lq * 4] = ph;
-        *(f16x4*)&pLo[w][bt * 16 + l15][nt * 16 + lq * 4] = pl;
-      }
-      ps += __shfl_xor(ps, 16);
-      ps += __shfl_xor(ps, 32);
-      lsum[bt] = lsum[bt] * sc[bt] + ps;
-      m[bt] = mnew;
-    }
-    __asm__ volatile("s_waitcnt lgkmcnt(0)" ::: "memory");
-    f16x8 avh[3], avl[3];
-#pragma unroll
-    for (int mt = 0; mt < 3; mt++) {
-      avh[mt] = *(const f16x8*)&vT[0][mt * 16 + l15][lq * 8];
-      avl[mt] = *(const f16x8*)&vT[1][mt * 16 + l15][lq * 8];
-    }
-    f16x8 pbh[2], pbl[2];
-#pragma unroll
-    for (int bt = 0; bt < 2; bt++) {
-      pbh[bt] = *(const f16x8*)&pHi[w][bt * 16 + l15][lq * 8];
-      pbl[bt] = *(const f16x8*)&pLo[w][bt * 16 + l15][lq * 8];
-    }
-#pragma unroll
-    for (int mt = 0; mt < 3; mt++)
-#pragma unroll
-      for (int bt = 0; bt < 2; bt++) {
-#pragma unroll
-        for (int j = 0; j < 4; j++) O[mt][bt][j] *= sc[bt];
-        f32x4 o = O[mt][bt];
-        o = __builtin_amdgcn_mfma_f32_16x16x32_f16(avh[mt], pbh[bt], o, 0, 0, 0);
-        o = __builtin_amdgcn_mfma_f32_16x16x32_f16(avh[mt], pbl[bt], o, 0, 0, 0);
-        o = __builtin_amdgcn_mfma_f32_16x16x32_f16(avl[mt], pbh[bt], o, 0, 0, 0);
-        O[mt][bt] = o;
-      }
-  }
-  const int pc = h * FCHUNK + chunk;
-  if (lq == 0) {
-#pragma unroll
-    for (int bt = 0; bt < 2; bt++) {
-      float* pm = part_ml + ((size_t)pc * BSZ + b0 + bt * 16 + l15) * 2;
-      pm[0] = m[bt];
-      pm[1] = lsum[bt];
-    }
-  }
-#pragma unroll
-  for (int mt = 0; mt < 3; mt++)
-#pragma unroll
-    for (int bt = 0; bt < 2; bt++) {
-      float* po = part_o + ((size_t)pc * BSZ + b0 + bt * 16 + l15) * 48 +
-                  mt * 16 + lq * 4;
-      *(f32x4*)po = O[mt][bt];
-    }
-}
-
-__global__ __launch_bounds__(64)
-void hopfield_combine(const float* __restrict__ part_ml,
-                      const float* __restrict__ part_o, float* __restrict__ dst) {
-  const int bh = blockIdx.x;
-  const int h = bh >> 7, b = bh & 127;
-  const int c = threadIdx.x;
-  __shared__ float w[64];
-  const float* pm = part_ml + ((size_t)(h * 64 + c) * BSZ + b) * 2;
-  const float mp = pm[0];
-  const float lp = pm[1];
-  float M = mp;
-#pragma unroll
-  for (int off = 32; off; off >>= 1) M = fmaxf(M, __shfl_xor(M, off));
-  const float wp = __expf(mp - M);
-  w[c] = wp;
-  float L = lp * wp;
-#pragma unroll
-  for (int off = 32; off; off >>= 1) L += __shfl_xor(L, off);
-  __syncthreads();
-  if (c < DH) {
-    float o = 0.f;
-    for (int p = 0; p < 64; p++)
-      o += part_o[((size_t)(h * 64 + p) * BSZ + b) * 48 + c] * w[p];
-    dst[(size_t)b * DMODEL + h * DH + c] = o / L;
+  const int wb = w >> 1, wn = w & 1;
+  const int sr = t >> 1, sh = t & 1;
+  f32x4 acc[4][4];
+#pragma unroll
+  for (int a = 0; a < 4; a++)
+#pragma unroll
+    for (int b = 0; b < 4; b++)
+#pragma unroll
+      for (int r = 0; r < 4; r++) acc[a][b][r] = 0.f;
+  for (int k0 = 0; k0 < DMODEL; k0 += 32) {
+    __syncthreads();
+    {
+      const size_t aoff = (size_t)(n0 + sr) * DMODEL + k0 + sh * 16;
+      f16x8 ah0 = *(const f16x8*)(mb_hi + aoff);
+      f16x8 ah1 = *(const f16x8*)(mb_hi + aoff + 8);
+      f16x8 al0 = *(const f16x8*)(mb_lo + aoff);
+      f16x8 al1 = *(const f16x8*)(mb_lo + aoff + 8);
+      *(f16x8*)&As[0][sr][sh * 16] = ah0;
+      *(f16x8*)&As[0][sr][sh * 16 + 8] = ah1;
+      *(f16x8*)&As[1][sr][sh * 16] = al0;
+      *(f16x8*)&As[1][sr][sh * 16 + 8] = al1;
+    }
+    {
+      const size_t boff = (size_t)sr * DMODEL + k0 + sh * 16;
+      f16x8 bh0 = *(const f16x8*)(rq_hi + boff);
+      f16x8 bh1 = *(const f16x8*)(rq_hi + boff + 8);
+      f16x8 bl0 = *(const f16x8*)(rq_lo + boff);
+      f16x8 bl1 = *(const f16x8*)(rq_lo + boff + 8);
+      *(f16x8*)&Bs[0][sr][sh * 16] = bh0;
+      *(f16x8*)&Bs[0][sr][sh * 16 + 8] = bh1;
+      *(f16x8*)&Bs[1][sr][sh * 16] = bl0;
+      *(f16x8*)&Bs[1][sr][sh * 16 + 8] = bl1;
+    }
+    __syncthreads();
+    f16x8 ah[4], al[4];
+#pragma unroll
+    for (int fn = 0; fn < 4; fn++) {
+      const int row = wn * 64 + fn * 16 + l15;
+      ah[fn] = *(const f16x8*)&As[0][row][lq * 8];
+      al[fn] = *(const f16x8*)&As[1][row][lq * 8];
+    }
+    f16x8 bh[4], bl[4];
+#pragma unroll
+    for (int fb = 0; fb < 4; fb++) {
+      const int row = wb * 64 + fb * 16 + l15;
+      bh[fb] = *(const f16x8*)&Bs[0][row][lq * 8];
+      bl[fb] = *(const f16x8*)&Bs[1][row][lq * 8];
+    }
+#pragma unroll
+    for (int fn = 0; fn < 4; fn++)
+#pragma unroll
+      for (int fb = 0; fb < 4; fb++) {
+        f32x4 a = acc[fn][fb];
+        a = __builtin_amdgcn_mfma_f32_16x16x32_f16(ah[fn], bh[fb], a, 0, 0, 0);
+        a = __builtin_amdgcn_mfma_f32_16x16x32_f16(ah[fn], bl[fb], a, 0, 0, 0);
+        a = __builtin_amdgcn_mfma_f32_16x16x32_f16(al[fn], bh[fb], a, 0, 0, 0);
+        acc[fn][fb] = a;
+      }
+  }
+#pragma unroll
+  for (int fn = 0; fn < 4; fn++) {
+    const int gn = n0 + wn * 64 + fn * 16 + lq * 4;
+    const float4 bi4 = *(const float4*)(binv + gn);
+    const float bi[4] = {bi4.x, bi4.y, bi4.z, bi4.w};
+#pragma unroll
+    for (int fb = 0; fb < 4; fb++) {
+      const int b = wb * 64 + fb * 16 + l15;
+      const float sa = 20.f * ainv[b];
+      f32x4 o;
+#pragma unroll
+      for (int r = 0; r < 4; r++) o[r] = acc[fn][fb][r] * sa * bi[r];
+      *(f32x4*)(out + (size_t)b * NTOT + gn) = o;
+    }
   }
 }
 
@@ -833,13 +872,18 @@
   float* out = (float*)d_out;
   float* logits = out + BSZ * 4;
 
+  float* part_ml = logits;
+  float* part_o  = logits + (size_t)NHEAD * FCHUNK * BSZ * 2;
+  float* scr     = logits + (size_t)NHEAD * FCHUNK * BSZ * 50;
+  float* xi   = scr;
+  float* conv = scr + 1 * (size_t)BSZ * DMODEL;
+  float* comb = scr + 2 * (size_t)BSZ * DMODEL;
+  float* h1   = scr + 3 * (size_t)BSZ * DMODEL;
+
   const size_t ND16 = (size_t)NTOT * DMODEL / 2;
-  const size_t PART = (size_t)NHEAD * FCHUNK * BSZ * (2 + 48);
-  const size_t fixed = 3 * NTOT + 768 + 4 * ND16 + 4 * (size_t)BSZ * DMODEL +
-                       4 * (size_t)BSZ * DMODEL / 2 +
-                       2 * (size_t)2 * DMODEL * DMODEL / 2 + 2 * DMODEL;
-  const bool fast = (fixed + 2 * ND16) * sizeof(float) <= ws_size;
-  const size_t nhpart = fast ? 2 * ND16 : PART;
+  const size_t smalls = 3 * NTOT + 512 + 4 * (size_t)BSZ * DMODEL / 2 +
+                        2 * (size_t)DMODEL * DMODEL + 2 * DMODEL;
+  const bool fast = (smalls + 6 * ND16) * sizeof(float) <= ws_size;
 
   float* ws = (float*)d_ws;
   size_t off = 0;
@@ -850,30 +894,26 @@
   float* q_mean  = alloc(128);
   float* q_rstd  = alloc(128);
   float* rq_inv  = alloc(128);
-  float* pad_    = alloc(384);
-  f16* k_hi = (f16*)alloc(ND16);
-  f16* k_lo = (f16*)alloc(ND16);
-  f16* v_hi = (f16*)alloc(ND16);
-  f16* v_lo = (f16*)alloc(ND16);
-  float* nhpart_base = alloc(nhpart);
-  f16* nh_hi = (f16*)nhpart_base;
-  f16* nh_lo = (f16*)(nhpart_base + ND16);
-  float* part_ml = nhpart_base;
-  float* part_o  = nhpart_base + (size_t)NHEAD * FCHUNK * BSZ * 2;
-  float* xi   = alloc((size_t)BSZ * DMODEL);
-  float* conv = alloc((size_t)BSZ * DMODEL);
-  float* comb = alloc((size_t)BSZ * DMODEL);
-  float* h1   = alloc((size_t)BSZ * DMODEL);
+  float* pad_    = alloc(128);
+  f16* big0 = (f16*)alloc(ND16);
+  f16* big1 = (f16*)alloc(ND16);
+  f16* big2 = (f16*)alloc(ND16);
+  f16* big3 = (f16*)alloc(ND16);
+  f16* big4 = fast ? (f16*)alloc(ND16) : nullptr;
+  f16* big5 = fast ? (f16*)alloc(ND16) : nullptr;
   f16* xi_hi = (f16*)alloc((size_t)BSZ * DMODEL / 2);
   f16* xi_lo = (f16*)alloc((size_t)BSZ * DMODEL / 2);
   f16* rq_hi = (f16*)alloc((size_t)BSZ * DMODEL / 2);
   f16* rq_lo = (f16*)alloc((size_t)BSZ * DMODEL / 2);
-  f16* Wc_hi = (f16*)alloc((size_t)2 * DMODEL * DMODEL / 2);
-  f16* Wc_lo = (f16*)alloc((size_t)2 * DMODEL * DMODEL / 2);
+  f16* Wc_hi = (f16*)alloc((size_t)DMODEL * DMODEL);
+  f16* Wc_lo = (f16*)alloc((size_t)DMODEL * DMODEL);
   float* biasc = alloc(2 * DMODEL);
-  f16* mb16_hi = (f16*)k_hi;
-  f16* mb16_lo = (f16*)k_lo;
   (void)in_sizes; (void)n_in; (void)out_size; (void)pad_;
+
+  f16* k_hi = big0;
+  f16* k_lo = big1;
+  f16* mb16_hi = big0;
+  f16* mb16_lo = big1;
 
   row_stats<<<NTOT / 4, 256, 0, stream>>>(mb, NTOT, mb_mean, mb_rstd, mb_l2i);
   row_stats<<<BSZ / 4, 256, 0, stream>>>(qe, BSZ, q_mean, q_rstd, nullptr);
@@ -882,26 +922,31 @@
                                              Wc_hi, Wc_lo, biasc);
 
   if (fast) {
-    split_ln<<<(NTOT * DMODEL / 8) / 256, 256, 0, stream>>>(
-        mb, mb_mean, mb_rstd, nh_hi, nh_lo);
-    proj_dual_v2<<<dim3(2 * DMODEL / 128, NTOT / 128), 256, 0, stream>>>(
-        nh_hi, nh_lo, Wc_hi, Wc_lo, biasc, k_hi, k_lo, v_hi, v_lo);
+    proj_dual_tr<<<dim3(2 * DMODEL / 128, NTOT / 128), 256, 0, stream>>>(
+        mb, mb_mean, mb_rstd, Wc_hi, Wc_lo, biasc,
+        k_hi, k_lo, big2, big3, big4, big5, 1);
   } else {
-    proj_dual_insplit<<<dim3(2 * DMODEL / 128, NTOT / 128), 256, 0, stream>>>(
-        mb, mb_mean, mb_rstd, Wc_hi, Wc_lo, biasc, k_hi, k_lo, v_hi, v_lo);
+    proj_dual_tr<<<dim3(2 * DMODEL / 128, NTOT / 128), 256, 0, stream>>>(
+        mb, mb_mean, mb_rstd, Wc_hi, Wc_lo, biasc,
+        k_hi, k_lo, nullptr, nullptr, big2, big3, 0);
   }
   ln_gemm_f32<<<dim3(DMODEL / 64, BSZ / 64), 256, 0, stream>>>(
       qe, q_mean, q_rstd, ln_qg, ln_qb, Wq, bq, xi);
+  split_xi_k<<<(BSZ * DMODEL / 4) / 256, 256, 0, stream>>>(xi, xi_hi, xi_lo);
 
   for (int r = 0; r < 6; r++) {
-    const int valIsK = (r != 5);
-    const f16* valHi = valIsK ? k_hi : v_hi;
-    const f16* valLo = valIsK ? k_lo : v_lo;
-    float* dst = (r == 5) ? conv : xi;
-    split_xi_k<<<96, 256, 0, stream>>>(xi, xi_hi, xi_lo);
-    flash_round<<<dim3(FCHUNK, NHEAD), 256, 0, stream>>>(
-        k_hi, k_lo, valHi, valLo, xi_hi, xi_lo, part_ml, part_o, valIsK);
-    hopfield_combine<<<BSZ * NHEAD, 64, 0, stream>>>(part_ml, part_o, dst);
+    const int fin = (r == 5);
+    if (fast) {
+      const f16* vtH = fin ? big4 : big2;
+      const f16* vtL = fin ? big5 : big3;
+      flash_direct<<<dim3(FCHUNK, NHEAD), 256, 0, stream>>>(
+          k_hi, k_lo, vtH, vtL, xi_hi, xi_lo, part_ml, part_o);
+    } else {
+      flash_staged<<<dim3(FCHUNK, NHEAD), 256, 0, stream>>>(
+          k_hi, k_lo, big2, big3, xi_hi, xi_lo, part_ml, part_o, !fin);
+    }
+    combine_v2<<<BSZ * NHEAD, 64, 0, stream>>>(part_ml, part_o, fin,
+                                               conv, xi_hi, xi_lo);
   }
 
   gemm_bias<<<dim3(DMODEL / 64, BSZ / 64), 256, 0, stream>>>(conv, Wo, bo, qe, comb, 0);
```

New measurement: 1.558 ms. +3.5%, slower.
